# Kernel optimization log

Hardware: AMD Instinct MI355X
Metric: run time of the kernel (lower is better)

Reference implementation:

```python
import jax, jax.numpy as jnp
import numpy as np
from jax import lax

N = 4096
E = 131072
C = 128
CH = [(128, 256), (256, 512), (512, 512), (512, 256), (256, 128)]


def setup_inputs() -> dict:
    key = jax.random.key(0)
    ks = jax.random.split(key, 16)
    inp = {}
    inp["x"] = jax.random.normal(ks[0], (N, C), jnp.float32)
    src = jax.random.randint(ks[1], (E,), 0, N)
    dst = jax.random.randint(ks[2], (E,), 0, N)
    inp["edge_index"] = jnp.stack([src, dst]).astype(jnp.int32)
    for i, (ci, co) in enumerate(CH):
        inp[f"theta{i}"] = jax.random.normal(ks[3 + i], (ci, co), jnp.float32) / np.float32(np.sqrt(ci))
        inp[f"b{i}"] = jax.random.normal(ks[8 + i], (co,), jnp.float32) * 0.02
    inp["p1"] = jax.random.normal(ks[13], (256,), jnp.float32)
    inp["p2"] = jax.random.normal(ks[14], (512,), jnp.float32)
    return inp


def gcn(x, W, theta, b):
    """GCNConv with edge weights, dense-adjacency form.
    A_hat = W + I (self loops, weight 1); deg = row-sum of A_hat;
    out[i] = sum_{(r->i)} d^-1/2[r] * w * d^-1/2[i] * (x@theta)[r] + b."""
    n = W.shape[0]
    A = W + jnp.eye(n, dtype=W.dtype)
    deg = A.sum(axis=1)
    dinv = jnp.where(deg > 0, lax.rsqrt(deg), 0.0)
    An = dinv[:, None] * A * dinv[None, :]
    return An.T @ (x @ theta) + b


def augment_adj(W):
    """add_self_loops -> spspmm(A, A) -> remove_self_loops, dense form."""
    n = W.shape[0]
    A = W + jnp.eye(n, dtype=W.dtype)
    A2 = A @ A
    return A2 * (1.0 - jnp.eye(n, dtype=W.dtype))


def topk_pool(x, W, p, k):
    """TopKPooling (ratio fixed via static k, single graph)."""
    score = jnp.tanh((x @ p) / jnp.linalg.norm(p))
    vals, perm = lax.top_k(score, k)
    xp = x[perm] * vals[:, None]
    Wp = W[perm][:, perm]  # filter_adj on surviving nodes
    return xp, Wp, perm


def reference(x, edge_index, theta0, theta1, theta2, theta3, theta4,
              b0, b1, b2, b3, b4, p1, p2):
    n = x.shape[0]
    # dense weighted adjacency from edge list (edge_weight = ones, duplicates sum)
    W = jnp.zeros((n, n), x.dtype).at[edge_index[0], edge_index[1]].add(1.0)

    # down block 0
    x0 = jax.nn.relu(gcn(x, W, theta0, b0))                 # [N, 256]
    x1, W1, perm1 = topk_pool(x0, augment_adj(W), p1, n // 2)
    # down block 1
    x1b = jax.nn.relu(gcn(x1, W1, theta1, b1))              # [N/2, 512]
    x2, W2, perm2 = topk_pool(x1b, augment_adj(W1), p2, n // 4)
    # bottleneck block
    xb = jax.nn.relu(gcn(x2, W2, theta2, b2))               # [N/4, 512]
    summary = xb.mean(axis=0, keepdims=True)                # global_mean_pool, 1 graph
    # up block (i=3): edges[1]=W1, res=x1b, perm2
    up1 = jnp.zeros_like(x1b).at[perm2].set(xb)
    xu = jax.nn.relu(gcn(x1b + up1, W1, theta3, b3))        # [N/2, 256]
    # up block (i=4): edges[0]=W, res=x0, perm1
    up0 = jnp.zeros_like(x0).at[perm1].set(xu)
    xout = jax.nn.relu(gcn(x0 + up0, W, theta4, b4))        # [N, 128]
    return xout, summary
```

## Files before the change

kernel.cpp:

```cpp
#include <hip/hip_runtime.h>

#define N0 4096
#define P1K 2048
#define P2K 1024
#define SPLITS 4

typedef short bf16x8 __attribute__((ext_vector_type(8)));
typedef float f32x4 __attribute__((ext_vector_type(4)));

__device__ __forceinline__ unsigned short f2bf(float f) {
  unsigned int u = __float_as_uint(f);
  unsigned int r = (u + 0x7fff + ((u >> 16) & 1)) >> 16;
  return (unsigned short)r;
}
__device__ __forceinline__ float bf2f(unsigned short h) {
  unsigned int u = ((unsigned int)h) << 16;
  return __uint_as_float(u);
}

__device__ __forceinline__ float blockReduceSum256(float v) {
  __shared__ float sh[16];
  int lane = threadIdx.x & 63;
  int w = threadIdx.x >> 6;
#pragma unroll
  for (int o = 32; o > 0; o >>= 1) v += __shfl_down(v, o, 64);
  __syncthreads();
  if (lane == 0) sh[w] = v;
  __syncthreads();
  float r = 0.f;
  if (threadIdx.x == 0) {
    int nw = (blockDim.x + 63) >> 6;
    for (int i = 0; i < nw; ++i) r += sh[i];
  }
  return r;
}

__device__ __forceinline__ int blockScanExclusive(int v, volatile int* wsums) {
  int lane = threadIdx.x & 63, w = threadIdx.x >> 6;
  int x = v;
#pragma unroll
  for (int o = 1; o < 64; o <<= 1) {
    int y = __shfl_up(x, o, 64);
    if (lane >= o) x += y;
  }
  if (lane == 63) wsums[w] = x;
  __syncthreads();
  if (threadIdx.x < 64) {
    int nw = blockDim.x >> 6;
    int s = (threadIdx.x < nw) ? wsums[threadIdx.x] : 0;
#pragma unroll
    for (int o = 1; o < 16; o <<= 1) {
      int y = __shfl_up(s, o, 64);
      if (lane >= o) s += y;
    }
    if (threadIdx.x < nw) wsums[threadIdx.x] = s;
  }
  __syncthreads();
  int base = (w > 0) ? wsums[w - 1] : 0;
  __syncthreads();
  return base + x - v;
}

__global__ void count_edges(const int* __restrict__ src, const int* __restrict__ dst,
                            int* __restrict__ co, int* __restrict__ ci, int E) {
  int e = blockIdx.x * blockDim.x + threadIdx.x;
  if (e >= E) return;
  atomicAdd(&co[src[e]], 1);
  atomicAdd(&ci[dst[e]], 1);
}

__global__ __launch_bounds__(1024) void exscan_dual(const int* __restrict__ co,
                                                    const int* __restrict__ ci,
                                                    int* __restrict__ optr,
                                                    int* __restrict__ iptr,
                                                    float* __restrict__ dinv0) {
  __shared__ int ls[1024];
  const int* cnt = blockIdx.x ? ci : co;
  int* ptr = blockIdx.x ? iptr : optr;
  int t = threadIdx.x;
  int v0 = cnt[t * 4], v1 = cnt[t * 4 + 1], v2 = cnt[t * 4 + 2], v3 = cnt[t * 4 + 3];
  int s = v0 + v1 + v2 + v3;
  ls[t] = s;
  __syncthreads();
  for (int off = 1; off < 1024; off <<= 1) {
    int x = (t >= off) ? ls[t - off] : 0;
    __syncthreads();
    ls[t] += x;
    __syncthreads();
  }
  int ex = (t > 0) ? ls[t - 1] : 0;
  ptr[t * 4]     = ex;
  ptr[t * 4 + 1] = ex + v0;
  ptr[t * 4 + 2] = ex + v0 + v1;
  ptr[t * 4 + 3] = ex + v0 + v1 + v2;
  if (t == 1023) ptr[4096] = ex + s;
  if (blockIdx.x == 0) {
    dinv0[t * 4]     = rsqrtf((float)v0 + 1.f);
    dinv0[t * 4 + 1] = rsqrtf((float)v1 + 1.f);
    dinv0[t * 4 + 2] = rsqrtf((float)v2 + 1.f);
    dinv0[t * 4 + 3] = rsqrtf((float)v3 + 1.f);
  }
}

__global__ void fill_edges(const int* __restrict__ src, const int* __restrict__ dst,
                           const int* __restrict__ optr, const int* __restrict__ iptr,
                           int* __restrict__ fo, int* __restrict__ fi,
                           int* __restrict__ odst, int* __restrict__ isrc, int E) {
  int e = blockIdx.x * blockDim.x + threadIdx.x;
  if (e >= E) return;
  int s = src[e], d = dst[e];
  odst[optr[s] + atomicAdd(&fo[s], 1)] = d;
  isrc[iptr[d] + atomicAdd(&fi[d], 1)] = s;
}

__global__ void conv_T_all(const float* __restrict__ t0, const float* __restrict__ t1,
                           const float* __restrict__ t2, const float* __restrict__ t3,
                           const float* __restrict__ t4,
                           unsigned short* __restrict__ o0h, unsigned short* __restrict__ o0l,
                           unsigned short* __restrict__ o1h, unsigned short* __restrict__ o1l,
                           unsigned short* __restrict__ o2, unsigned short* __restrict__ o3,
                           unsigned short* __restrict__ o4) {
  int idx = blockIdx.x * 256 + threadIdx.x;
  if (idx < 32768) {
    int k = idx >> 8, n = idx & 255;
    float v = t0[idx];
    unsigned short h = f2bf(v);
    o0h[(size_t)n * 128 + k] = h;
    o0l[(size_t)n * 128 + k] = f2bf(v - bf2f(h));
  } else if (idx < 163840) {
    int i = idx - 32768;
    int k = i >> 9, n = i & 511;
    float v = t1[i];
    unsigned short h = f2bf(v);
    o1h[(size_t)n * 256 + k] = h;
    o1l[(size_t)n * 256 + k] = f2bf(v - bf2f(h));
  } else if (idx < 425984) {
    int i = idx - 163840;
    int k = i >> 9, n = i & 511;
    o2[(size_t)n * 512 + k] = f2bf(t2[i]);
  } else if (idx < 557056) {
    int i = idx - 425984;
    int k = i >> 8, n = i & 255;
    o3[(size_t)n * 512 + k] = f2bf(t3[i]);
  } else if (idx < 589824) {
    int i = idx - 557056;
    int k = i >> 7, n = i & 127;
    o4[(size_t)n * 256 + k] = f2bf(t4[i]);
  }
}

template <bool TOUT>
__global__ __launch_bounds__(256) void gemm3(const float* __restrict__ A,
                                             const unsigned short* __restrict__ BhT,
                                             const unsigned short* __restrict__ BlT,
                                             const int* __restrict__ permA,
                                             const float* __restrict__ valsA,
                                             const float* __restrict__ dinv,
                                             float* __restrict__ C,
                                             unsigned short* __restrict__ ChT,
                                             unsigned short* __restrict__ ClT,
                                             int M, int N, int K, int nbx) {
  __shared__ unsigned short U[16384];
  unsigned short* Ah = U;
  unsigned short* Al = U + 4096;
  unsigned short* Bh = U + 8192;
  unsigned short* Bl = U + 12288;
  int tid = threadIdx.x;
  int by = blockIdx.x / nbx, bx = blockIdx.x % nbx;
  int row0 = by << 6, col0 = bx << 6;
  int l = tid & 63, wv = tid >> 6;
  int wr = (wv >> 1) << 5, wc = (wv & 1) << 5;
  f32x4 acc[2][2] = {};
  for (int k0 = 0; k0 < K; k0 += 64) {
#pragma unroll
    for (int it = 0; it < 2; ++it) {
      int idx = (it << 8) + tid;
      int r = idx >> 3, c8 = idx & 7;
      int sw = c8 ^ (r & 7);
      int row = row0 + r;
      int srow = permA ? permA[row] : row;
      float vs = valsA ? valsA[row] : 1.f;
      const float* Af = A + (size_t)srow * K + k0 + (c8 << 3);
      float4 f0 = *(const float4*)Af;
      float4 f1 = *(const float4*)(Af + 4);
      float vv[8] = {f0.x * vs, f0.y * vs, f0.z * vs, f0.w * vs,
                     f1.x * vs, f1.y * vs, f1.z * vs, f1.w * vs};
      uint4 uh, ul;
      unsigned short hh[8], ll[8];
#pragma unroll
      for (int q = 0; q < 8; ++q) {
        hh[q] = f2bf(vv[q]);
        ll[q] = f2bf(vv[q] - bf2f(hh[q]));
      }
      uh.x = (unsigned)hh[0] | ((unsigned)hh[1] << 16);
      uh.y = (unsigned)hh[2] | ((unsigned)hh[3] << 16);
      uh.z = (unsigned)hh[4] | ((unsigned)hh[5] << 16);
      uh.w = (unsigned)hh[6] | ((unsigned)hh[7] << 16);
      ul.x = (unsigned)ll[0] | ((unsigned)ll[1] << 16);
      ul.y = (unsigned)ll[2] | ((unsigned)ll[3] << 16);
      ul.z = (unsigned)ll[4] | ((unsigned)ll[5] << 16);
      ul.w = (unsigned)ll[6] | ((unsigned)ll[7] << 16);
      ((uint4*)Ah)[(r << 3) + sw] = uh;
      ((uint4*)Al)[(r << 3) + sw] = ul;
      ((uint4*)Bh)[(r << 3) + sw] =
          *(const uint4*)(BhT + (size_t)(col0 + r) * K + k0 + (c8 << 3));
      ((uint4*)Bl)[(r << 3) + sw] =
          *(const uint4*)(BlT + (size_t)(col0 + r) * K + k0 + (c8 << 3));
    }
    __syncthreads();
#pragma unroll
    for (int kk2 = 0; kk2 < 2; ++kk2) {
      int ch = (kk2 << 2) + (l >> 4);
      int ra = wr + (l & 15), rb = ra + 16;
      int ca = wc + (l & 15), cb = ca + 16;
      int oa0 = (ra << 6) + ((ch ^ (ra & 7)) << 3);
      int oa1 = (rb << 6) + ((ch ^ (rb & 7)) << 3);
      int ob0 = (ca << 6) + ((ch ^ (ca & 7)) << 3);
      int ob1 = (cb << 6) + ((ch ^ (cb & 7)) << 3);
      bf16x8 ah0 = *(const bf16x8*)&Ah[oa0], ah1 = *(const bf16x8*)&Ah[oa1];
      bf16x8 al0 = *(const bf16x8*)&Al[oa0], al1 = *(const bf16x8*)&Al[oa1];
      bf16x8 bh0 = *(const bf16x8*)&Bh[ob0], bh1 = *(const bf16x8*)&Bh[ob1];
      bf16x8 bl0 = *(const bf16x8*)&Bl[ob0], bl1 = *(const bf16x8*)&Bl[ob1];
      acc[0][0] = __builtin_amdgcn_mfma_f32_16x16x32_bf16(ah0, bh0, acc[0][0], 0, 0, 0);
      acc[0][1] = __builtin_amdgcn_mfma_f32_16x16x32_bf16(ah0, bh1, acc[0][1], 0, 0, 0);
      acc[1][0] = __builtin_amdgcn_mfma_f32_16x16x32_bf16(ah1, bh0, acc[1][0], 0, 0, 0);
      acc[1][1] = __builtin_amdgcn_mfma_f32_16x16x32_bf16(ah1, bh1, acc[1][1], 0, 0, 0);
      acc[0][0] = __builtin_amdgcn_mfma_f32_16x16x32_bf16(ah0, bl0, acc[0][0], 0, 0, 0);
      acc[0][1] = __builtin_amdgcn_mfma_f32_16x16x32_bf16(ah0, bl1, acc[0][1], 0, 0, 0);
      acc[1][0] = __builtin_amdgcn_mfma_f32_16x16x32_bf16(ah1, bl0, acc[1][0], 0, 0, 0);
      acc[1][1] = __builtin_amdgcn_mfma_f32_16x16x32_bf16(ah1, bl1, acc[1][1], 0, 0, 0);
      acc[0][0] = __builtin_amdgcn_mfma_f32_16x16x32_bf16(al0, bh0, acc[0][0], 0, 0, 0);
      acc[0][1] = __builtin_amdgcn_mfma_f32_16x16x32_bf16(al0, bh1, acc[0][1], 0, 0, 0);
      acc[1][0] = __builtin_amdgcn_mfma_f32_16x16x32_bf16(al1, bh0, acc[1][0], 0, 0, 0);
      acc[1][1] = __builtin_amdgcn_mfma_f32_16x16x32_bf16(al1, bh1, acc[1][1], 0, 0, 0);
    }
    __syncthreads();
  }
  int lrow = (l >> 4) << 2, lcol = l & 15;
  float* tf = (float*)U;
#pragma unroll
  for (int i = 0; i < 2; ++i)
#pragma unroll
    for (int j = 0; j < 2; ++j) {
      int lc = wc + (j << 4) + lcol;
      int lr0 = wr + (i << 4) + lrow;
      int c = col0 + lc;
#pragma unroll
      for (int rg = 0; rg < 4; ++rg) {
        int lr = lr0 + rg;
        int r = row0 + lr;
        float dv = dinv ? dinv[r] : 1.f;
        float v = acc[i][j][rg] * dv;
        C[(size_t)r * N + c] = v;
        if (TOUT) tf[lr * 65 + lc] = v;
      }
    }
  if (TOUT) {
    __syncthreads();
    for (int it = 0; it < 16; ++it) {
      int idx = (it << 8) + tid;
      int rr = idx >> 6, cc = idx & 63;
      float v = tf[cc * 65 + rr];
      unsigned short h = f2bf(v);
      size_t o = (size_t)(col0 + rr) * M + row0 + cc;
      ChT[o] = h;
      ClT[o] = f2bf(v - bf2f(h));
    }
  }
}

template <bool ABF16>
__global__ __launch_bounds__(256) void gemm_sk(const void* __restrict__ Av,
                                               const unsigned short* __restrict__ BT,
                                               const int* __restrict__ permA,
                                               const float* __restrict__ valsA,
                                               float* __restrict__ Pf,
                                               int M, int N, int K, int nbx, int nb2d) {
  __shared__ unsigned short As[64 * 64];
  __shared__ unsigned short Bs[64 * 64];
  int tid = threadIdx.x;
  int s = blockIdx.x / nb2d;
  int r2 = blockIdx.x % nb2d;
  int by = r2 / nbx, bx = r2 % nbx;
  int row0 = by << 6, col0 = bx << 6;
  int kc = K / SPLITS;
  int ks = s * kc, ke = ks + kc;
  int l = tid & 63, wv = tid >> 6;
  int wr = (wv >> 1) << 5, wc = (wv & 1) << 5;
  f32x4 acc[2][2] = {};
  for (int k0 = ks; k0 < ke; k0 += 64) {
#pragma unroll
    for (int it = 0; it < 2; ++it) {
      int idx = (it << 8) + tid;
      int r = idx >> 3, c8 = idx & 7;
      int sw = c8 ^ (r & 7);
      if (ABF16) {
        ((uint4*)As)[(r << 3) + sw] =
            *(const uint4*)((const unsigned short*)Av + (size_t)(row0 + r) * K + k0 + (c8 << 3));
      } else {
        int row = row0 + r;
        int srow = permA ? permA[row] : row;
        float vs = valsA ? valsA[row] : 1.f;
        const float* Af = (const float*)Av + (size_t)srow * K + k0 + (c8 << 3);
        float4 f0 = *(const float4*)Af;
        float4 f1 = *(const float4*)(Af + 4);
        uint4 u;
        u.x = (unsigned)f2bf(f0.x * vs) | ((unsigned)f2bf(f0.y * vs) << 16);
        u.y = (unsigned)f2bf(f0.z * vs) | ((unsigned)f2bf(f0.w * vs) << 16);
        u.z = (unsigned)f2bf(f1.x * vs) | ((unsigned)f2bf(f1.y * vs) << 16);
        u.w = (unsigned)f2bf(f1.z * vs) | ((unsigned)f2bf(f1.w * vs) << 16);
        ((uint4*)As)[(r << 3) + sw] = u;
      }
      ((uint4*)Bs)[(r << 3) + sw] =
          *(const uint4*)(BT + (size_t)(col0 + r) * K + k0 + (c8 << 3));
    }
    __syncthreads();
#pragma unroll
    for (int kk2 = 0; kk2 < 2; ++kk2) {
      int ch = (kk2 << 2) + (l >> 4);
      int ra = wr + (l & 15), rb = ra + 16;
      int ca = wc + (l & 15), cb = ca + 16;
      bf16x8 a0 = *(const bf16x8*)&As[(ra << 6) + ((ch ^ (ra & 7)) << 3)];
      bf16x8 a1 = *(const bf16x8*)&As[(rb << 6) + ((ch ^ (rb & 7)) << 3)];
      bf16x8 b0 = *(const bf16x8*)&Bs[(ca << 6) + ((ch ^ (ca & 7)) << 3)];
      bf16x8 b1 = *(const bf16x8*)&Bs[(cb << 6) + ((ch ^ (cb & 7)) << 3)];
      acc[0][0] = __builtin_amdgcn_mfma_f32_16x16x32_bf16(a0, b0, acc[0][0], 0, 0, 0);
      acc[0][1] = __builtin_amdgcn_mfma_f32_16x16x32_bf16(a0, b1, acc[0][1], 0, 0, 0);
      acc[1][0] = __builtin_amdgcn_mfma_f32_16x16x32_bf16(a1, b0, acc[1][0], 0, 0, 0);
      acc[1][1] = __builtin_amdgcn_mfma_f32_16x16x32_bf16(a1, b1, acc[1][1], 0, 0, 0);
    }
    __syncthreads();
  }
  int lrow = (l >> 4) << 2, lcol = l & 15;
  float* P = Pf + (size_t)s * M * N;
#pragma unroll
  for (int i = 0; i < 2; ++i)
#pragma unroll
    for (int j = 0; j < 2; ++j) {
      int c = col0 + wc + (j << 4) + lcol;
      int r0 = row0 + wr + (i << 4) + lrow;
#pragma unroll
      for (int rg = 0; rg < 4; ++rg)
        P[(size_t)(r0 + rg) * N + c] = acc[i][j][rg];
    }
}

__global__ __launch_bounds__(256) void gemm_skd(const unsigned short* __restrict__ A,
                                                const unsigned short* __restrict__ BhT,
                                                const unsigned short* __restrict__ BlT,
                                                float* __restrict__ Pf,
                                                int M, int N, int K, int nbx, int nb2d) {
  __shared__ unsigned short As[4096], Bh[4096], Bl[4096];
  int tid = threadIdx.x;
  int s = blockIdx.x / nb2d;
  int r2 = blockIdx.x % nb2d;
  int by = r2 / nbx, bx = r2 % nbx;
  int row0 = by << 6, col0 = bx << 6;
  int kc = K / SPLITS;
  int ks = s * kc, ke = ks + kc;
  int l = tid & 63, wv = tid >> 6;
  int wr = (wv >> 1) << 5, wc = (wv & 1) << 5;
  f32x4 acc[2][2] = {};
  for (int k0 = ks; k0 < ke; k0 += 64) {
#pragma unroll
    for (int it = 0; it < 2; ++it) {
      int idx = (it << 8) + tid;
      int r = idx >> 3, c8 = idx & 7;
      int sw = c8 ^ (r & 7);
      ((uint4*)As)[(r << 3) + sw] =
          *(const uint4*)(A + (size_t)(row0 + r) * K + k0 + (c8 << 3));
      ((uint4*)Bh)[(r << 3) + sw] =
          *(const uint4*)(BhT + (size_t)(col0 + r) * K + k0 + (c8 << 3));
      ((uint4*)Bl)[(r << 3) + sw] =
          *(const uint4*)(BlT + (size_t)(col0 + r) * K + k0 + (c8 << 3));
    }
    __syncthreads();
#pragma unroll
    for (int kk2 = 0; kk2 < 2; ++kk2) {
      int ch = (kk2 << 2) + (l >> 4);
      int ra = wr + (l & 15), rb = ra + 16;
      int ca = wc + (l & 15), cb = ca + 16;
      bf16x8 a0 = *(const bf16x8*)&As[(ra << 6) + ((ch ^ (ra & 7)) << 3)];
      bf16x8 a1 = *(const bf16x8*)&As[(rb << 6) + ((ch ^ (rb & 7)) << 3)];
      bf16x8 bh0 = *(const bf16x8*)&Bh[(ca << 6) + ((ch ^ (ca & 7)) << 3)];
      bf16x8 bh1 = *(const bf16x8*)&Bh[(cb << 6) + ((ch ^ (cb & 7)) << 3)];
      bf16x8 bl0 = *(const bf16x8*)&Bl[(ca << 6) + ((ch ^ (ca & 7)) << 3)];
      bf16x8 bl1 = *(const bf16x8*)&Bl[(cb << 6) + ((ch ^ (cb & 7)) << 3)];
      acc[0][0] = __builtin_amdgcn_mfma_f32_16x16x32_bf16(a0, bh0, acc[0][0], 0, 0, 0);
      acc[0][1] = __builtin_amdgcn_mfma_f32_16x16x32_bf16(a0, bh1, acc[0][1], 0, 0, 0);
      acc[1][0] = __builtin_amdgcn_mfma_f32_16x16x32_bf16(a1, bh0, acc[1][0], 0, 0, 0);
      acc[1][1] = __builtin_amdgcn_mfma_f32_16x16x32_bf16(a1, bh1, acc[1][1], 0, 0, 0);
      acc[0][0] = __builtin_amdgcn_mfma_f32_16x16x32_bf16(a0, bl0, acc[0][0], 0, 0, 0);
      acc[0][1] = __builtin_amdgcn_mfma_f32_16x16x32_bf16(a0, bl1, acc[0][1], 0, 0, 0);
      acc[1][0] = __builtin_amdgcn_mfma_f32_16x16x32_bf16(a1, bl0, acc[1][0], 0, 0, 0);
      acc[1][1] = __builtin_amdgcn_mfma_f32_16x16x32_bf16(a1, bl1, acc[1][1], 0, 0, 0);
    }
    __syncthreads();
  }
  int lrow = (l >> 4) << 2, lcol = l & 15;
  float* P = Pf + (size_t)s * M * N;
#pragma unroll
  for (int i = 0; i < 2; ++i)
#pragma unroll
    for (int j = 0; j < 2; ++j) {
      int c = col0 + wc + (j << 4) + lcol;
      int r0 = row0 + wr + (i << 4) + lrow;
#pragma unroll
      for (int rg = 0; rg < 4; ++rg)
        P[(size_t)(r0 + rg) * N + c] = acc[i][j][rg];
    }
}

__global__ __launch_bounds__(256) void epi_red0_t(const float* __restrict__ Pf,
                                                  const float* __restrict__ dinv,
                                                  float* __restrict__ Cf,
                                                  unsigned short* __restrict__ CbT,
                                                  int M, int N, int dm) {
  __shared__ float t[64][65];
  int nbx = N >> 6;
  int by = blockIdx.x / nbx, bx = blockIdx.x % nbx;
  int r0 = by << 6, c0 = bx << 6;
  size_t MN = (size_t)M * N;
  for (int it = 0; it < 16; ++it) {
    int idx = (it << 8) + threadIdx.x;
    int r = idx >> 6, c = idx & 63;
    size_t o = (size_t)(r0 + r) * N + c0 + c;
    float v = 0.f;
#pragma unroll
    for (int s = 0; s < SPLITS; ++s) v += Pf[s * MN + o];
    float dv = 1.f;
    if (dm == 1) dv = dinv[r0 + r];
    else if (dm == 2) dv = rsqrtf(dinv[r0 + r] + 1.f);
    v *= dv;
    Cf[o] = v;
    t[r][c] = v;
  }
  __syncthreads();
  if (CbT) {
    for (int it = 0; it < 16; ++it) {
      int idx = (it << 8) + threadIdx.x;
      int rr = idx >> 6, cc = idx & 63;
      CbT[(size_t)(c0 + rr) * M + r0 + cc] = f2bf(t[cc][rr]);
    }
  }
}

__global__ __launch_bounds__(256) void epi_red1(const float* __restrict__ Pf,
                                                const float* __restrict__ Zadd,
                                                const float* __restrict__ dinv,
                                                const float* __restrict__ bias,
                                                const int* __restrict__ permS,
                                                float* __restrict__ scatterDst,
                                                float* __restrict__ outp, int M, int N,
                                                int dm) {
  int g = blockIdx.x * 256 + threadIdx.x;
  size_t base = (size_t)g * 4;
  size_t MN = (size_t)M * N;
  if (base >= MN) return;
  int r = (int)(base / N), c = (int)(base % N);
  float4 a = *(const float4*)&Pf[base];
#pragma unroll
  for (int s = 1; s < SPLITS; ++s) {
    float4 p = *(const float4*)&Pf[s * MN + base];
    a.x += p.x; a.y += p.y; a.z += p.z; a.w += p.w;
  }
  float4 z = *(const float4*)&Zadd[base];
  float dv = (dm == 2) ? rsqrtf(dinv[r] + 1.f) : dinv[r];
  float4 bb = *(const float4*)&bias[c];
  float4 o;
  o.x = fmaxf(dv * (a.x + z.x) + bb.x, 0.f);
  o.y = fmaxf(dv * (a.y + z.y) + bb.y, 0.f);
  o.z = fmaxf(dv * (a.z + z.z) + bb.z, 0.f);
  o.w = fmaxf(dv * (a.w + z.w) + bb.w, 0.f);
  if (outp) *(float4*)&outp[base] = o;
  if (permS) {
    float4* d = (float4*)&scatterDst[(size_t)permS[r] * N + c];
    float4 cur = *d;
    cur.x += o.x; cur.y += o.y; cur.z += o.z; cur.w += o.w;
    *d = cur;
  }
}

__global__ __launch_bounds__(256) void epi_red1s(const float* __restrict__ Pf,
                                                 const float* __restrict__ Zadd,
                                                 const float* __restrict__ dinv,
                                                 const float* __restrict__ bias,
                                                 const float* __restrict__ pvec,
                                                 float* __restrict__ sc,
                                                 float* __restrict__ outp) {
  __shared__ float shs[2][2][2];
  int li = threadIdx.x & 127;
  int lr = threadIdx.x >> 7;
  int r = blockIdx.x * 2 + lr;
  size_t base = (size_t)r * 512 + li * 4;
  const size_t MN = (size_t)2048 * 512;
  float4 a = *(const float4*)&Pf[base];
#pragma unroll
  for (int s = 1; s < SPLITS; ++s) {
    float4 p = *(const float4*)&Pf[s * MN + base];
    a.x += p.x; a.y += p.y; a.z += p.z; a.w += p.w;
  }
  float4 z = *(const float4*)&Zadd[base];
  float dv = dinv[r];
  float4 bb = *(const float4*)&bias[li * 4];
  float4 o;
  o.x = fmaxf(dv * (a.x + z.x) + bb.x, 0.f);
  o.y = fmaxf(dv * (a.y + z.y) + bb.y, 0.f);
  o.z = fmaxf(dv * (a.z + z.z) + bb.z, 0.f);
  o.w = fmaxf(dv * (a.w + z.w) + bb.w, 0.f);
  *(float4*)&outp[base] = o;
  float4 pv = *(const float4*)&pvec[li * 4];
  float s1 = pv.x * pv.x + pv.y * pv.y + pv.z * pv.z + pv.w * pv.w;
  float s2 = o.x * pv.x + o.y * pv.y + o.z * pv.z + o.w * pv.w;
#pragma unroll
  for (int t = 32; t > 0; t >>= 1) {
    s1 += __shfl_down(s1, t, 64);
    s2 += __shfl_down(s2, t, 64);
  }
  int wir = (threadIdx.x >> 6) & 1;
  if ((threadIdx.x & 63) == 0) { shs[lr][wir][0] = s1; shs[lr][wir][1] = s2; }
  __syncthreads();
  if ((threadIdx.x & 127) == 0) {
    float S1 = shs[lr][0][0] + shs[lr][1][0];
    float S2 = shs[lr][0][1] + shs[lr][1][1];
    sc[r] = tanhf(S2 / sqrtf(S1));
  }
}

__global__ __launch_bounds__(256) void mm_w2_mfma(const unsigned short* __restrict__ Wb,
                                                  const unsigned short* __restrict__ WbT,
                                                  const int* __restrict__ perm2,
                                                  float* __restrict__ W2f) {
  __shared__ unsigned short As[64 * 64];
  __shared__ unsigned short Bs[64 * 64];
  __shared__ int pr[64], pc[64];
  int tid = threadIdx.x;
  int s = blockIdx.x >> 8;
  int t2d = blockIdx.x & 255;
  int bx = t2d & 15, by = t2d >> 4;
  int row0 = by << 6, col0 = bx << 6;
  int ks = s * 512, ke = ks + 512;
  if (tid < 64) pr[tid] = perm2[row0 + tid];
  else if (tid < 128) pc[tid - 64] = perm2[col0 + tid - 128 + 64];
  __syncthreads();
  int l = tid & 63, wv = tid >> 6;
  int wr = (wv >> 1) << 5, wc = (wv & 1) << 5;
  f32x4 acc[2][2] = {};
  for (int k0 = ks; k0 < ke; k0 += 64) {
#pragma unroll
    for (int it = 0; it < 2; ++it) {
      int idx = (it << 8) + tid;
      int r = idx >> 3, c8 = idx & 7;
      int sw = c8 ^ (r & 7);
      ((uint4*)As)[(r << 3) + sw] =
          *(const uint4*)(Wb + (size_t)pr[r] * 2048 + k0 + (c8 << 3));
      ((uint4*)Bs)[(r << 3) + sw] =
          *(const uint4*)(WbT + (size_t)pc[r] * 2048 + k0 + (c8 << 3));
    }
    __syncthreads();
    if (tid < 64) {
      int r = tid, d = pr[r] - k0;
      if (d >= 0 && d < 64) {
        int ui = (r << 6) + (((d >> 3) ^ (r & 7)) << 3) + (d & 7);
        As[ui] = f2bf(bf2f(As[ui]) + 1.f);
      }
    } else if (tid < 128) {
      int c = tid - 64, d = pc[c] - k0;
      if (d >= 0 && d < 64) {
        int ui = (c << 6) + (((d >> 3) ^ (c & 7)) << 3) + (d & 7);
        Bs[ui] = f2bf(bf2f(Bs[ui]) + 1.f);
      }
    }
    __syncthreads();
#pragma unroll
    for (int kk2 = 0; kk2 < 2; ++kk2) {
      int ch = (kk2 << 2) + (l >> 4);
      int ra = wr + (l & 15), rb = ra + 16;
      int ca = wc + (l & 15), cb = ca + 16;
      bf16x8 a0 = *(const bf16x8*)&As[(ra << 6) + ((ch ^ (ra & 7)) << 3)];
      bf16x8 a1 = *(const bf16x8*)&As[(rb << 6) + ((ch ^ (rb & 7)) << 3)];
      bf16x8 b0 = *(const bf16x8*)&Bs[(ca << 6) + ((ch ^ (ca & 7)) << 3)];
      bf16x8 b1 = *(const bf16x8*)&Bs[(cb << 6) + ((ch ^ (cb & 7)) << 3)];
      acc[0][0] = __builtin_amdgcn_mfma_f32_16x16x32_bf16(a0, b0, acc[0][0], 0, 0, 0);
      acc[0][1] = __builtin_amdgcn_mfma_f32_16x16x32_bf16(a0, b1, acc[0][1], 0, 0, 0);
      acc[1][0] = __builtin_amdgcn_mfma_f32_16x16x32_bf16(a1, b0, acc[1][0], 0, 0, 0);
      acc[1][1] = __builtin_amdgcn_mfma_f32_16x16x32_bf16(a1, b1, acc[1][1], 0, 0, 0);
    }
    __syncthreads();
  }
  int lrow = (l >> 4) << 2, lcol = l & 15;
#pragma unroll
  for (int i = 0; i < 2; ++i)
#pragma unroll
    for (int j = 0; j < 2; ++j) {
      int c = col0 + wc + (j << 4) + lcol;
      int r0 = row0 + wr + (i << 4) + lrow;
#pragma unroll
      for (int rg = 0; rg < 4; ++rg)
        atomicAdd(&W2f[(size_t)(r0 + rg) * 1024 + c], acc[i][j][rg]);
    }
}

__global__ __launch_bounds__(256) void w2_post(const float* __restrict__ W2f,
                                               unsigned short* __restrict__ W2Tb,
                                               float* __restrict__ degsum2) {
  __shared__ float t[64][65];
  int bx = blockIdx.x & 15, by = blockIdx.x >> 4;
  int r0 = by << 6, c0 = bx << 6;
  for (int it = 0; it < 16; ++it) {
    int idx = (it << 8) + threadIdx.x;
    int r = idx >> 6, c = idx & 63;
    float v = W2f[(size_t)(r0 + r) * 1024 + c0 + c];
    if (r0 + r == c0 + c) v = 0.f;
    t[r][c] = v;
  }
  __syncthreads();
  if (threadIdx.x < 64) {
    float s = 0.f;
    for (int c = 0; c < 64; ++c) s += t[threadIdx.x][c];
    atomicAdd(&degsum2[r0 + threadIdx.x], s);
  }
  for (int it = 0; it < 16; ++it) {
    int idx = (it << 8) + threadIdx.x;
    int rr = idx >> 6, cc = idx & 63;
    W2Tb[(size_t)(c0 + rr) * 1024 + r0 + cc] = f2bf(t[cc][rr]);
  }
}

__global__ __launch_bounds__(256) void transpose_bf16(const unsigned short* __restrict__ in,
                                                      unsigned short* __restrict__ out,
                                                      int n) {
  __shared__ unsigned short t[64][65];
  int nb = n >> 6;
  int bx = blockIdx.x % nb, by = blockIdx.x / nb;
  int r0 = by << 6, c0 = bx << 6;
  for (int it = 0; it < 16; ++it) {
    int idx = (it << 8) + threadIdx.x;
    int r = idx >> 6, c = idx & 63;
    t[r][c] = in[(size_t)(r0 + r) * n + c0 + c];
  }
  __syncthreads();
  for (int it = 0; it < 16; ++it) {
    int idx = (it << 8) + threadIdx.x;
    int r = idx >> 6, c = idx & 63;
    out[(size_t)(c0 + r) * n + r0 + c] = t[c][r];
  }
}

template <int C, bool SCORE>
__global__ __launch_bounds__(256) void gcn_spmm4(const int* __restrict__ iptr,
                                                 const int* __restrict__ isrc,
                                                 const float* __restrict__ Z,
                                                 const float* __restrict__ dinv,
                                                 const float* __restrict__ bias,
                                                 const float* __restrict__ pvec,
                                                 float* __restrict__ sc,
                                                 float* __restrict__ outp) {
  constexpr int L = C / 4;
  int li = threadIdx.x % L;
  int i = blockIdx.x * (256 / L) + threadIdx.x / L;
  float4 acc = *(const float4*)(Z + (size_t)i * C + li * 4);
  int beg = iptr[i], end = iptr[i + 1];
  for (int e = beg; e < end; ++e) {
    float4 z = *(const float4*)(Z + (size_t)isrc[e] * C + li * 4);
    acc.x += z.x; acc.y += z.y; acc.z += z.z; acc.w += z.w;
  }
  float d = dinv[i];
  float4 bb = *(const float4*)(bias + li * 4);
  float4 o;
  o.x = fmaxf(d * acc.x + bb.x, 0.f);
  o.y = fmaxf(d * acc.y + bb.y, 0.f);
  o.z = fmaxf(d * acc.z + bb.z, 0.f);
  o.w = fmaxf(d * acc.w + bb.w, 0.f);
  *(float4*)(outp + (size_t)i * C + li * 4) = o;
  if (SCORE) {
    float4 pv = *(const float4*)(pvec + li * 4);
    float s1 = pv.x * pv.x + pv.y * pv.y + pv.z * pv.z + pv.w * pv.w;
    float s2 = o.x * pv.x + o.y * pv.y + o.z * pv.z + o.w * pv.w;
#pragma unroll
    for (int t = 32; t > 0; t >>= 1) {
      s1 += __shfl_down(s1, t, 64);
      s2 += __shfl_down(s2, t, 64);
    }
    if ((threadIdx.x & 63) == 0) sc[i] = tanhf(s2 / sqrtf(s1));
  }
}

__global__ __launch_bounds__(1024) void topk_select(const float* __restrict__ score,
                                                    int n, int k, int* __restrict__ perm,
                                                    float* __restrict__ vals,
                                                    int* __restrict__ rank) {
  __shared__ unsigned int keys[4096];
  __shared__ int hist[256];
  __shared__ int wsums[16];
  __shared__ unsigned int sh_prefix;
  __shared__ int sh_rem;
  int t = threadIdx.x;
  int m = n >> 10;
  for (int i = t; i < n; i += 1024) {
    unsigned int u = __float_as_uint(score[i]);
    keys[i] = u ^ ((unsigned int)((int)u >> 31) | 0x80000000u);
  }
  if (t == 0) { sh_prefix = 0u; sh_rem = k; }
  __syncthreads();
  for (int round = 0; round < 4; ++round) {
    int shift = 24 - (round << 3);
    if (t < 256) hist[t] = 0;
    __syncthreads();
    unsigned int prefix = sh_prefix;
    unsigned int maskhi = (round == 0) ? 0u : (0xFFFFFFFFu << (shift + 8));
    for (int i = t; i < n; i += 1024) {
      unsigned int kk = keys[i];
      if ((kk & maskhi) == prefix) atomicAdd(&hist[(kk >> shift) & 255], 1);
    }
    __syncthreads();
    if (t == 0) {
      int rem = sh_rem, acc = 0, b = 255;
      for (; b > 0; --b) {
        if (acc + hist[b] >= rem) break;
        acc += hist[b];
      }
      sh_rem = rem - acc;
      sh_prefix = prefix | ((unsigned int)b << shift);
    }
    __syncthreads();
  }
  unsigned int thr = sh_prefix;
  int need = sh_rem;
  int base = t * m;
  int f[4];
  int cnt = 0;
#pragma unroll
  for (int j = 0; j < 4; ++j) {
    f[j] = 0;
    if (j < m) { f[j] = (keys[base + j] == thr) ? 1 : 0; cnt += f[j]; }
  }
  int ex = blockScanExclusive(cnt, wsums);
  int sel[4];
  int scnt = 0;
#pragma unroll
  for (int j = 0; j < 4; ++j) {
    sel[j] = 0;
    if (j < m) {
      unsigned int kk = keys[base + j];
      sel[j] = (kk > thr) || (kk == thr && ex < need);
      ex += f[j];
      scnt += sel[j];
    }
  }
  int pos = blockScanExclusive(scnt, wsums);
#pragma unroll
  for (int j = 0; j < 4; ++j) {
    if (j < m) {
      int i = base + j;
      if (sel[j]) {
        unsigned int kk = keys[i];
        unsigned int u = (kk & 0x80000000u) ? (kk ^ 0x80000000u) : ~kk;
        perm[pos] = i;
        vals[pos] = __uint_as_float(u);
        rank[i] = pos;
        pos++;
      } else {
        rank[i] = -1;
      }
    }
  }
}

__global__ __launch_bounds__(256) void build_W1(const int* __restrict__ optr,
                                                const int* __restrict__ odst,
                                                const int* __restrict__ perm1,
                                                const int* __restrict__ rank1,
                                                unsigned short* __restrict__ W1b,
                                                float* __restrict__ dinv1) {
  __shared__ float row[2048];
  int a = blockIdx.x;
  int pa = perm1[a];
  for (int i = threadIdx.x; i < 2048; i += 256) row[i] = 0.f;
  __syncthreads();
  int kbeg = optr[pa], kend = optr[pa + 1];
  int nk = kend - kbeg + 1;
  int wv = threadIdx.x >> 6, lane = threadIdx.x & 63;
  for (int kidx = wv; kidx < nk; kidx += 4) {
    int k = (kidx == 0) ? pa : odst[kbeg + kidx - 1];
    int jbeg = optr[k], jend = optr[k + 1];
    for (int jj = jbeg - 1 + lane; jj < jend; jj += 64) {
      int j = (jj < jbeg) ? k : odst[jj];
      int rb = rank1[j];
      if (rb >= 0) atomicAdd(&row[rb], 1.0f);
    }
  }
  __syncthreads();
  float ssum = 0.f;
  for (int i = threadIdx.x; i < 2048; i += 256) {
    float v = (i == a) ? 0.f : row[i];
    W1b[(size_t)a * 2048 + i] = f2bf(v);
    ssum += v;
  }
  float t = blockReduceSum256(ssum);
  if (threadIdx.x == 0) dinv1[a] = rsqrtf(t + 1.0f);
}

__global__ void mean_cols(const float* __restrict__ X, int R, int C, float* __restrict__ outp) {
  int c = blockIdx.x;
  float s = 0.f;
  for (int r = threadIdx.x; r < R; r += blockDim.x) s += X[(size_t)r * C + c];
  float t = blockReduceSum256(s);
  if (threadIdx.x == 0) outp[c] = t / (float)R;
}

extern "C" void kernel_launch(void* const* d_in, const int* in_sizes, int n_in,
                              void* d_out, int out_size, void* d_ws, size_t ws_size,
                              hipStream_t stream) {
  const float* x      = (const float*)d_in[0];
  const int*   eidx   = (const int*)d_in[1];
  const float* theta0 = (const float*)d_in[2];
  const float* b0     = (const float*)d_in[3];
  const float* theta1 = (const float*)d_in[4];
  const float* b1     = (const float*)d_in[5];
  const float* theta2 = (const float*)d_in[6];
  const float* b2     = (const float*)d_in[7];
  const float* theta3 = (const float*)d_in[8];
  const float* b3     = (const float*)d_in[9];
  const float* theta4 = (const float*)d_in[10];
  const float* b4     = (const float*)d_in[11];
  const float* p1     = (const float*)d_in[12];
  const float* p2     = (const float*)d_in[13];
  const int E = in_sizes[1] / 2;
  const int* src = eidx;
  const int* dst = eidx + E;
  float* out = (float*)d_out;

  char* wsb = (char*)d_ws;
  size_t off = 0;
  auto alloc = [&](size_t bytes) -> void* {
    void* p = wsb + off;
    off = (off + bytes + 255) & ~(size_t)255;
    return p;
  };
  char* zblock = (char*)alloc((size_t)4 * N0 * 4 + P2K * 4 + (size_t)P2K * P2K * 4);
  int* cnt4 = (int*)zblock;
  float* degsum2 = (float*)(zblock + (size_t)4 * N0 * 4);
  float* W2f = (float*)(zblock + (size_t)4 * N0 * 4 + P2K * 4);
  size_t zbytes = (size_t)4 * N0 * 4 + P2K * 4 + (size_t)P2K * P2K * 4;

  int* optr  = (int*)alloc((N0 + 1) * 4);
  int* iptr  = (int*)alloc((N0 + 1) * 4);
  int* odst  = (int*)alloc((size_t)E * 4);
  int* isrc  = (int*)alloc((size_t)E * 4);
  int* perm1 = (int*)alloc(P1K * 4);
  int* rank1 = (int*)alloc(N0 * 4);
  int* perm2 = (int*)alloc(P2K * 4);
  int* rank2 = (int*)alloc(P1K * 4);
  float* dinv0 = (float*)alloc(N0 * 4);
  float* dinv1 = (float*)alloc(P1K * 4);
  float* vals1 = (float*)alloc(P1K * 4);
  float* vals2 = (float*)alloc(P2K * 4);
  float* score = (float*)alloc(N0 * 4);
  float* x0  = (float*)alloc((size_t)N0 * 256 * 4);
  float* x1b = (float*)alloc((size_t)P1K * 512 * 4);
  float* xb  = (float*)alloc((size_t)P2K * 512 * 4);
  float* SA  = (float*)alloc((size_t)P1K * 512 * 4);
  float* Pf  = (float*)alloc((size_t)SPLITS * 1048576 * 4);
  unsigned short* W1b  = (unsigned short*)alloc((size_t)P1K * P1K * 2);
  unsigned short* W1bT = (unsigned short*)alloc((size_t)P1K * P1K * 2);
  unsigned short* W2Tb = (unsigned short*)alloc((size_t)P2K * P2K * 2);
  unsigned short* SAbT = (unsigned short*)alloc((size_t)524288 * 2);
  unsigned short* ZhT  = (unsigned short*)alloc((size_t)512 * 2048 * 2);
  unsigned short* ZlT  = (unsigned short*)alloc((size_t)512 * 2048 * 2);
  unsigned short* t0hT = (unsigned short*)alloc((size_t)256 * 128 * 2);
  unsigned short* t0lT = (unsigned short*)alloc((size_t)256 * 128 * 2);
  unsigned short* t1hT = (unsigned short*)alloc((size_t)512 * 256 * 2);
  unsigned short* t1lT = (unsigned short*)alloc((size_t)512 * 256 * 2);
  unsigned short* t2T  = (unsigned short*)alloc((size_t)512 * 512 * 2);
  unsigned short* t3T  = (unsigned short*)alloc((size_t)256 * 512 * 2);
  unsigned short* t4T  = (unsigned short*)alloc((size_t)128 * 256 * 2);
  (void)ws_size; (void)n_in; (void)out_size;

  int* co = cnt4;
  int* ci = cnt4 + N0;
  int* fo = cnt4 + 2 * N0;
  int* fi = cnt4 + 3 * N0;

  hipMemsetAsync(zblock, 0, zbytes, stream);
  count_edges<<<E / 256, 256, 0, stream>>>(src, dst, co, ci, E);
  exscan_dual<<<2, 1024, 0, stream>>>(co, ci, optr, iptr, dinv0);
  fill_edges<<<E / 256, 256, 0, stream>>>(src, dst, optr, iptr, fo, fi, odst, isrc, E);
  conv_T_all<<<2304, 256, 0, stream>>>(theta0, theta1, theta2, theta3, theta4,
                                       t0hT, t0lT, t1hT, t1lT, t2T, t3T, t4T);

  gemm3<false><<<64 * 4, 256, 0, stream>>>(x, t0hT, t0lT, nullptr, nullptr, dinv0, SA,
                                           nullptr, nullptr, 4096, 256, 128, 4);
  gcn_spmm4<256, true><<<1024, 256, 0, stream>>>(iptr, isrc, SA, dinv0, b0, p1, score, x0);

  topk_select<<<1, 1024, 0, stream>>>(score, 4096, 2048, perm1, vals1, rank1);
  build_W1<<<2048, 256, 0, stream>>>(optr, odst, perm1, rank1, W1b, dinv1);
  transpose_bf16<<<(2048 / 64) * (2048 / 64), 256, 0, stream>>>(W1b, W1bT, 2048);

  gemm3<true><<<32 * 8, 256, 0, stream>>>(x0, t1hT, t1lT, perm1, vals1, dinv1, SA,
                                          ZhT, ZlT, 2048, 512, 256, 8);
  gemm_skd<<<256 * SPLITS, 256, 0, stream>>>(W1bT, ZhT, ZlT, Pf, 2048, 512, 2048, 8, 256);
  epi_red1s<<<1024, 256, 0, stream>>>(Pf, SA, dinv1, b1, p2, score, x1b);

  topk_select<<<1, 1024, 0, stream>>>(score, 2048, 1024, perm2, vals2, rank2);
  mm_w2_mfma<<<256 * SPLITS, 256, 0, stream>>>(W1b, W1bT, perm2, W2f);
  w2_post<<<256, 256, 0, stream>>>(W2f, W2Tb, degsum2);

  gemm_sk<false><<<128 * SPLITS, 256, 0, stream>>>(x1b, t2T, perm2, vals2, Pf,
                                                   1024, 512, 512, 8, 128);
  epi_red0_t<<<128, 256, 0, stream>>>(Pf, degsum2, SA, SAbT, 1024, 512, 2);
  gemm_sk<true><<<128 * SPLITS, 256, 0, stream>>>(W2Tb, SAbT, nullptr, nullptr, Pf,
                                                  1024, 512, 1024, 8, 128);
  epi_red1<<<1024 * 512 / 1024, 256, 0, stream>>>(Pf, SA, degsum2, b2, perm2, x1b, xb,
                                                  1024, 512, 2);
  mean_cols<<<512, 256, 0, stream>>>(xb, 1024, 512, out + 524288);

  gemm_sk<false><<<128 * SPLITS, 256, 0, stream>>>(x1b, t3T, nullptr, nullptr, Pf,
                                                   2048, 256, 512, 4, 128);
  epi_red0_t<<<128, 256, 0, stream>>>(Pf, dinv1, SA, SAbT, 2048, 256, 1);
  gemm_sk<true><<<128 * SPLITS, 256, 0, stream>>>(W1bT, SAbT, nullptr, nullptr, Pf,
                                                  2048, 256, 2048, 4, 128);
  epi_red1<<<2048 * 256 / 1024, 256, 0, stream>>>(Pf, SA, dinv1, b3, perm1, x0, nullptr,
                                                  2048, 256, 1);

  gemm_sk<false><<<128 * SPLITS, 256, 0, stream>>>(x0, t4T, nullptr, nullptr, Pf,
                                                   4096, 128, 256, 2, 128);
  epi_red0_t<<<128, 256, 0, stream>>>(Pf, dinv0, SA, nullptr, 4096, 128, 1);
  gcn_spmm4<128, false><<<512, 256, 0, stream>>>(iptr, isrc, SA, dinv0, b4, nullptr, nullptr,
                                                 out);
}
```

Before: 331.3 us.

## Fuse independent kernels via block-index dispatch and drop split-K for small GEMMs

Independent stages are merged into single launches that pick their work by block index: edge counting with the theta conversion, edge fill with the first GEMM, the transpose with the second GEMM, the W2 product with the bottleneck feature GEMM, and the column mean with the up-block feature GEMM. The small feature GEMMs that used split-K plus a separate reduction/epilogue kernel now use a non-split GEMM with the dinv scaling and transposed bf16 output fused into the epilogue, and a new w2T kernel produces dinv2 directly. This removes many launches and partial-sum round trips through memory. In exchange, mixed-role kernels carry the larger shared-memory and register footprint of their heaviest body, which can lower occupancy, and the non-split GEMMs launch fewer blocks.

```diff
diff --git a/kernel.cpp b/kernel.cpp
--- a/kernel.cpp
+++ b/kernel.cpp
@@ -61,66 +61,30 @@
   return base + x - v;
 }
 
-__global__ void count_edges(const int* __restrict__ src, const int* __restrict__ dst,
-                            int* __restrict__ co, int* __restrict__ ci, int E) {
-  int e = blockIdx.x * blockDim.x + threadIdx.x;
-  if (e >= E) return;
-  atomicAdd(&co[src[e]], 1);
-  atomicAdd(&ci[dst[e]], 1);
-}
-
-__global__ __launch_bounds__(1024) void exscan_dual(const int* __restrict__ co,
-                                                    const int* __restrict__ ci,
-                                                    int* __restrict__ optr,
-                                                    int* __restrict__ iptr,
-                                                    float* __restrict__ dinv0) {
-  __shared__ int ls[1024];
-  const int* cnt = blockIdx.x ? ci : co;
-  int* ptr = blockIdx.x ? iptr : optr;
-  int t = threadIdx.x;
-  int v0 = cnt[t * 4], v1 = cnt[t * 4 + 1], v2 = cnt[t * 4 + 2], v3 = cnt[t * 4 + 3];
-  int s = v0 + v1 + v2 + v3;
-  ls[t] = s;
-  __syncthreads();
-  for (int off = 1; off < 1024; off <<= 1) {
-    int x = (t >= off) ? ls[t - off] : 0;
-    __syncthreads();
-    ls[t] += x;
-    __syncthreads();
-  }
-  int ex = (t > 0) ? ls[t - 1] : 0;
-  ptr[t * 4]     = ex;
-  ptr[t * 4 + 1] = ex + v0;
-  ptr[t * 4 + 2] = ex + v0 + v1;
-  ptr[t * 4 + 3] = ex + v0 + v1 + v2;
-  if (t == 1023) ptr[4096] = ex + s;
-  if (blockIdx.x == 0) {
-    dinv0[t * 4]     = rsqrtf((float)v0 + 1.f);
-    dinv0[t * 4 + 1] = rsqrtf((float)v1 + 1.f);
-    dinv0[t * 4 + 2] = rsqrtf((float)v2 + 1.f);
-    dinv0[t * 4 + 3] = rsqrtf((float)v3 + 1.f);
-  }
-}
-
-__global__ void fill_edges(const int* __restrict__ src, const int* __restrict__ dst,
-                           const int* __restrict__ optr, const int* __restrict__ iptr,
-                           int* __restrict__ fo, int* __restrict__ fi,
-                           int* __restrict__ odst, int* __restrict__ isrc, int E) {
-  int e = blockIdx.x * blockDim.x + threadIdx.x;
-  if (e >= E) return;
-  int s = src[e], d = dst[e];
-  odst[optr[s] + atomicAdd(&fo[s], 1)] = d;
-  isrc[iptr[d] + atomicAdd(&fi[d], 1)] = s;
-}
-
-__global__ void conv_T_all(const float* __restrict__ t0, const float* __restrict__ t1,
-                           const float* __restrict__ t2, const float* __restrict__ t3,
-                           const float* __restrict__ t4,
-                           unsigned short* __restrict__ o0h, unsigned short* __restrict__ o0l,
-                           unsigned short* __restrict__ o1h, unsigned short* __restrict__ o1l,
-                           unsigned short* __restrict__ o2, unsigned short* __restrict__ o3,
-                           unsigned short* __restrict__ o4) {
-  int idx = blockIdx.x * 256 + threadIdx.x;
+__device__ __forceinline__ void count_edges_body(int b, const int* __restrict__ src,
+                                                 const int* __restrict__ dst,
+                                                 int* __restrict__ co, int* __restrict__ ci,
+                                                 int E) {
+  int e = b * 256 + threadIdx.x;
+  if (e < E) {
+    atomicAdd(&co[src[e]], 1);
+    atomicAdd(&ci[dst[e]], 1);
+  }
+}
+
+__device__ __forceinline__ void conv_body(int b, const float* __restrict__ t0,
+                                          const float* __restrict__ t1,
+                                          const float* __restrict__ t2,
+                                          const float* __restrict__ t3,
+                                          const float* __restrict__ t4,
+                                          unsigned short* __restrict__ o0h,
+                                          unsigned short* __restrict__ o0l,
+                                          unsigned short* __restrict__ o1h,
+                                          unsigned short* __restrict__ o1l,
+                                          unsigned short* __restrict__ o2,
+                                          unsigned short* __restrict__ o3,
+                                          unsigned short* __restrict__ o4) {
+  int idx = b * 256 + threadIdx.x;
   if (idx < 32768) {
     int k = idx >> 8, n = idx & 255;
     float v = t0[idx];
@@ -149,24 +113,79 @@
   }
 }
 
+__global__ __launch_bounds__(256) void fused_ce_conv(
+    const int* __restrict__ src, const int* __restrict__ dst, int* __restrict__ co,
+    int* __restrict__ ci, int E, const float* t0, const float* t1, const float* t2,
+    const float* t3, const float* t4, unsigned short* o0h, unsigned short* o0l,
+    unsigned short* o1h, unsigned short* o1l, unsigned short* o2, unsigned short* o3,
+    unsigned short* o4) {
+  if (blockIdx.x < 512) count_edges_body(blockIdx.x, src, dst, co, ci, E);
+  else conv_body(blockIdx.x - 512, t0, t1, t2, t3, t4, o0h, o0l, o1h, o1l, o2, o3, o4);
+}
+
+__global__ __launch_bounds__(1024) void exscan_dual(const int* __restrict__ co,
+                                                    const int* __restrict__ ci,
+                                                    int* __restrict__ optr,
+                                                    int* __restrict__ iptr,
+                                                    float* __restrict__ dinv0) {
+  __shared__ int ls[1024];
+  const int* cnt = blockIdx.x ? ci : co;
+  int* ptr = blockIdx.x ? iptr : optr;
+  int t = threadIdx.x;
+  int v0 = cnt[t * 4], v1 = cnt[t * 4 + 1], v2 = cnt[t * 4 + 2], v3 = cnt[t * 4 + 3];
+  int s = v0 + v1 + v2 + v3;
+  ls[t] = s;
+  __syncthreads();
+  for (int off = 1; off < 1024; off <<= 1) {
+    int x = (t >= off) ? ls[t - off] : 0;
+    __syncthreads();
+    ls[t] += x;
+    __syncthreads();
+  }
+  int ex = (t > 0) ? ls[t - 1] : 0;
+  ptr[t * 4]     = ex;
+  ptr[t * 4 + 1] = ex + v0;
+  ptr[t * 4 + 2] = ex + v0 + v1;
+  ptr[t * 4 + 3] = ex + v0 + v1 + v2;
+  if (t == 1023) ptr[4096] = ex + s;
+  if (blockIdx.x == 0) {
+    dinv0[t * 4]     = rsqrtf((float)v0 + 1.f);
+    dinv0[t * 4 + 1] = rsqrtf((float)v1 + 1.f);
+    dinv0[t * 4 + 2] = rsqrtf((float)v2 + 1.f);
+    dinv0[t * 4 + 3] = rsqrtf((float)v3 + 1.f);
+  }
+}
+
+__device__ __forceinline__ void fill_body(int b, const int* __restrict__ src,
+                                          const int* __restrict__ dst,
+                                          const int* __restrict__ optr,
+                                          const int* __restrict__ iptr,
+                                          int* __restrict__ fo, int* __restrict__ fi,
+                                          int* __restrict__ odst, int* __restrict__ isrc,
+                                          int E) {
+  int e = b * 256 + threadIdx.x;
+  if (e < E) {
+    int s = src[e], d = dst[e];
+    odst[optr[s] + atomicAdd(&fo[s], 1)] = d;
+    isrc[iptr[d] + atomicAdd(&fi[d], 1)] = s;
+  }
+}
+
 template <bool TOUT>
-__global__ __launch_bounds__(256) void gemm3(const float* __restrict__ A,
-                                             const unsigned short* __restrict__ BhT,
-                                             const unsigned short* __restrict__ BlT,
-                                             const int* __restrict__ permA,
-                                             const float* __restrict__ valsA,
-                                             const float* __restrict__ dinv,
-                                             float* __restrict__ C,
-                                             unsigned short* __restrict__ ChT,
-                                             unsigned short* __restrict__ ClT,
-                                             int M, int N, int K, int nbx) {
+__device__ void gemm3_body(int bid, const float* __restrict__ A,
+                           const unsigned short* __restrict__ BhT,
+                           const unsigned short* __restrict__ BlT,
+                           const int* __restrict__ permA, const float* __restrict__ valsA,
+                           const float* __restrict__ dinv, float* __restrict__ C,
+                           unsigned short* __restrict__ ChT, unsigned short* __restrict__ ClT,
+                           int M, int N, int K, int nbx) {
   __shared__ unsigned short U[16384];
   unsigned short* Ah = U;
   unsigned short* Al = U + 4096;
   unsigned short* Bh = U + 8192;
   unsigned short* Bl = U + 12288;
   int tid = threadIdx.x;
-  int by = blockIdx.x / nbx, bx = blockIdx.x % nbx;
+  int by = bid / nbx, bx = bid % nbx;
   int row0 = by << 6, col0 = bx << 6;
   int l = tid & 63, wv = tid >> 6;
   int wr = (wv >> 1) << 5, wc = (wv & 1) << 5;
@@ -269,80 +288,42 @@
   }
 }
 
-template <bool ABF16>
-__global__ __launch_bounds__(256) void gemm_sk(const void* __restrict__ Av,
-                                               const unsigned short* __restrict__ BT,
-                                               const int* __restrict__ permA,
-                                               const float* __restrict__ valsA,
-                                               float* __restrict__ Pf,
-                                               int M, int N, int K, int nbx, int nb2d) {
-  __shared__ unsigned short As[64 * 64];
-  __shared__ unsigned short Bs[64 * 64];
-  int tid = threadIdx.x;
-  int s = blockIdx.x / nb2d;
-  int r2 = blockIdx.x % nb2d;
-  int by = r2 / nbx, bx = r2 % nbx;
-  int row0 = by << 6, col0 = bx << 6;
-  int kc = K / SPLITS;
-  int ks = s * kc, ke = ks + kc;
-  int l = tid & 63, wv = tid >> 6;
-  int wr = (wv >> 1) << 5, wc = (wv & 1) << 5;
-  f32x4 acc[2][2] = {};
-  for (int k0 = ks; k0 < ke; k0 += 64) {
-#pragma unroll
-    for (int it = 0; it < 2; ++it) {
-      int idx = (it << 8) + tid;
-      int r = idx >> 3, c8 = idx & 7;
-      int sw = c8 ^ (r & 7);
-      if (ABF16) {
-        ((uint4*)As)[(r << 3) + sw] =
-            *(const uint4*)((const unsigned short*)Av + (size_t)(row0 + r) * K + k0 + (c8 << 3));
-      } else {
-        int row = row0 + r;
-        int srow = permA ? permA[row] : row;
-        float vs = valsA ? valsA[row] : 1.f;
-        const float* Af = (const float*)Av + (size_t)srow * K + k0 + (c8 << 3);
-        float4 f0 = *(const float4*)Af;
-        float4 f1 = *(const float4*)(Af + 4);
-        uint4 u;
-        u.x = (unsigned)f2bf(f0.x * vs) | ((unsigned)f2bf(f0.y * vs) << 16);
-        u.y = (unsigned)f2bf(f0.z * vs) | ((unsigned)f2bf(f0.w * vs) << 16);
-        u.z = (unsigned)f2bf(f1.x * vs) | ((unsigned)f2bf(f1.y * vs) << 16);
-        u.w = (unsigned)f2bf(f1.z * vs) | ((unsigned)f2bf(f1.w * vs) << 16);
-        ((uint4*)As)[(r << 3) + sw] = u;
-      }
-      ((uint4*)Bs)[(r << 3) + sw] =
-          *(const uint4*)(BT + (size_t)(col0 + r) * K + k0 + (c8 << 3));
-    }
-    __syncthreads();
-#pragma unroll
-    for (int kk2 = 0; kk2 < 2; ++kk2) {
-      int ch = (kk2 << 2) + (l >> 4);
-      int ra = wr + (l & 15), rb = ra + 16;
-      int ca = wc + (l & 15), cb = ca + 16;
-      bf16x8 a0 = *(const bf16x8*)&As[(ra << 6) + ((ch ^ (ra & 7)) << 3)];
-      bf16x8 a1 = *(const bf16x8*)&As[(rb << 6) + ((ch ^ (rb & 7)) << 3)];
-      bf16x8 b0 = *(const bf16x8*)&Bs[(ca << 6) + ((ch ^ (ca & 7)) << 3)];
-      bf16x8 b1 = *(const bf16x8*)&Bs[(cb << 6) + ((ch ^ (cb & 7)) << 3)];
-      acc[0][0] = __builtin_amdgcn_mfma_f32_16x16x32_bf16(a0, b0, acc[0][0], 0, 0, 0);
-      acc[0][1] = __builtin_amdgcn_mfma_f32_16x16x32_bf16(a0, b1, acc[0][1], 0, 0, 0);
-      acc[1][0] = __builtin_amdgcn_mfma_f32_16x16x32_bf16(a1, b0, acc[1][0], 0, 0, 0);
-      acc[1][1] = __builtin_amdgcn_mfma_f32_16x16x32_bf16(a1, b1, acc[1][1], 0, 0, 0);
-    }
-    __syncthreads();
-  }
-  int lrow = (l >> 4) << 2, lcol = l & 15;
-  float* P = Pf + (size_t)s * M * N;
-#pragma unroll
-  for (int i = 0; i < 2; ++i)
-#pragma unroll
-    for (int j = 0; j < 2; ++j) {
-      int c = col0 + wc + (j << 4) + lcol;
-      int r0 = row0 + wr + (i << 4) + lrow;
-#pragma unroll
-      for (int rg = 0; rg < 4; ++rg)
-        P[(size_t)(r0 + rg) * N + c] = acc[i][j][rg];
-    }
+__global__ __launch_bounds__(256) void fused_fill_g3(
+    const int* src, const int* dst, const int* optr, const int* iptr, int* fo, int* fi,
+    int* odst, int* isrc, int E, const float* x, const unsigned short* t0hT,
+    const unsigned short* t0lT, const float* dinv0, float* SA) {
+  if (blockIdx.x < 512) fill_body(blockIdx.x, src, dst, optr, iptr, fo, fi, odst, isrc, E);
+  else gemm3_body<false>(blockIdx.x - 512, x, t0hT, t0lT, nullptr, nullptr, dinv0, SA,
+                         nullptr, nullptr, 4096, 256, 128, 4);
+}
+
+__device__ void transpose_body(int bid, const unsigned short* __restrict__ in,
+                               unsigned short* __restrict__ out, int n) {
+  __shared__ unsigned short t[64][65];
+  int nb = n >> 6;
+  int bx = bid % nb, by = bid / nb;
+  int r0 = by << 6, c0 = bx << 6;
+  for (int it = 0; it < 16; ++it) {
+    int idx = (it << 8) + threadIdx.x;
+    int r = idx >> 6, c = idx & 63;
+    t[r][c] = in[(size_t)(r0 + r) * n + c0 + c];
+  }
+  __syncthreads();
+  for (int it = 0; it < 16; ++it) {
+    int idx = (it << 8) + threadIdx.x;
+    int r = idx >> 6, c = idx & 63;
+    out[(size_t)(c0 + r) * n + r0 + c] = t[c][r];
+  }
+}
+
+__global__ __launch_bounds__(256) void fused_tr_g3(
+    const unsigned short* W1b, unsigned short* W1bT, const float* x0,
+    const unsigned short* t1hT, const unsigned short* t1lT, const int* perm1,
+    const float* vals1, const float* dinv1, float* SA, unsigned short* ZhT,
+    unsigned short* ZlT) {
+  if (blockIdx.x < 1024) transpose_body(blockIdx.x, W1b, W1bT, 2048);
+  else gemm3_body<true>(blockIdx.x - 1024, x0, t1hT, t1lT, perm1, vals1, dinv1, SA,
+                        ZhT, ZlT, 2048, 512, 256, 8);
 }
 
 __global__ __launch_bounds__(256) void gemm_skd(const unsigned short* __restrict__ A,
@@ -411,37 +392,276 @@
     }
 }
 
-__global__ __launch_bounds__(256) void epi_red0_t(const float* __restrict__ Pf,
-                                                  const float* __restrict__ dinv,
-                                                  float* __restrict__ Cf,
-                                                  unsigned short* __restrict__ CbT,
-                                                  int M, int N, int dm) {
+__global__ __launch_bounds__(256) void gemm_sk(const unsigned short* __restrict__ A,
+                                               const unsigned short* __restrict__ BT,
+                                               float* __restrict__ Pf,
+                                               int M, int N, int K, int nbx, int nb2d) {
+  __shared__ unsigned short As[4096];
+  __shared__ unsigned short Bs[4096];
+  int tid = threadIdx.x;
+  int s = blockIdx.x / nb2d;
+  int r2 = blockIdx.x % nb2d;
+  int by = r2 / nbx, bx = r2 % nbx;
+  int row0 = by << 6, col0 = bx << 6;
+  int kc = K / SPLITS;
+  int ks = s * kc, ke = ks + kc;
+  int l = tid & 63, wv = tid >> 6;
+  int wr = (wv >> 1) << 5, wc = (wv & 1) << 5;
+  f32x4 acc[2][2] = {};
+  for (int k0 = ks; k0 < ke; k0 += 64) {
+#pragma unroll
+    for (int it = 0; it < 2; ++it) {
+      int idx = (it << 8) + tid;
+      int r = idx >> 3, c8 = idx & 7;
+      int sw = c8 ^ (r & 7);
+      ((uint4*)As)[(r << 3) + sw] =
+          *(const uint4*)(A + (size_t)(row0 + r) * K + k0 + (c8 << 3));
+      ((uint4*)Bs)[(r << 3) + sw] =
+          *(const uint4*)(BT + (size_t)(col0 + r) * K + k0 + (c8 << 3));
+    }
+    __syncthreads();
+#pragma unroll
+    for (int kk2 = 0; kk2 < 2; ++kk2) {
+      int ch = (kk2 << 2) + (l >> 4);
+      int ra = wr + (l & 15), rb = ra + 16;
+      int ca = wc + (l & 15), cb = ca + 16;
+      bf16x8 a0 = *(const bf16x8*)&As[(ra << 6) + ((ch ^ (ra & 7)) << 3)];
+      bf16x8 a1 = *(const bf16x8*)&As[(rb << 6) + ((ch ^ (rb & 7)) << 3)];
+      bf16x8 b0 = *(const bf16x8*)&Bs[(ca << 6) + ((ch ^ (ca & 7)) << 3)];
+      bf16x8 b1 = *(const bf16x8*)&Bs[(cb << 6) + ((ch ^ (cb & 7)) << 3)];
+      acc[0][0] = __builtin_amdgcn_mfma_f32_16x16x32_bf16(a0, b0, acc[0][0], 0, 0, 0);
+      acc[0][1] = __builtin_amdgcn_mfma_f32_16x16x32_bf16(a0, b1, acc[0][1], 0, 0, 0);
+      acc[1][0] = __builtin_amdgcn_mfma_f32_16x16x32_bf16(a1, b0, acc[1][0], 0, 0, 0);
+      acc[1][1] = __builtin_amdgcn_mfma_f32_16x16x32_bf16(a1, b1, acc[1][1], 0, 0, 0);
+    }
+    __syncthreads();
+  }
+  int lrow = (l >> 4) << 2, lcol = l & 15;
+  float* P = Pf + (size_t)s * M * N;
+#pragma unroll
+  for (int i = 0; i < 2; ++i)
+#pragma unroll
+    for (int j = 0; j < 2; ++j) {
+      int c = col0 + wc + (j << 4) + lcol;
+      int r0 = row0 + wr + (i << 4) + lrow;
+#pragma unroll
+      for (int rg = 0; rg < 4; ++rg)
+        P[(size_t)(r0 + rg) * N + c] = acc[i][j][rg];
+    }
+}
+
+__device__ void gemm_e_body(int bid, const float* __restrict__ A,
+                            const unsigned short* __restrict__ BT,
+                            const int* __restrict__ permA, const float* __restrict__ valsA,
+                            const float* __restrict__ dinv, int dm,
+                            float* __restrict__ Cf, unsigned short* __restrict__ CbT,
+                            int M, int N, int K, int nbx) {
+  __shared__ char gsm[16640];
+  unsigned short* As = (unsigned short*)gsm;
+  unsigned short* Bs = (unsigned short*)(gsm + 8192);
+  int tid = threadIdx.x;
+  int by = bid / nbx, bx = bid % nbx;
+  int row0 = by << 6, col0 = bx << 6;
+  int l = tid & 63, wv = tid >> 6;
+  int wr = (wv >> 1) << 5, wc = (wv & 1) << 5;
+  f32x4 acc[2][2] = {};
+  for (int k0 = 0; k0 < K; k0 += 64) {
+#pragma unroll
+    for (int it = 0; it < 2; ++it) {
+      int idx = (it << 8) + tid;
+      int r = idx >> 3, c8 = idx & 7;
+      int sw = c8 ^ (r & 7);
+      int row = row0 + r;
+      int srow = permA ? permA[row] : row;
+      float vs = valsA ? valsA[row] : 1.f;
+      const float* Af = A + (size_t)srow * K + k0 + (c8 << 3);
+      float4 f0 = *(const float4*)Af;
+      float4 f1 = *(const float4*)(Af + 4);
+      uint4 u;
+      u.x = (unsigned)f2bf(f0.x * vs) | ((unsigned)f2bf(f0.y * vs) << 16);
+      u.y = (unsigned)f2bf(f0.z * vs) | ((unsigned)f2bf(f0.w * vs) << 16);
+      u.z = (unsigned)f2bf(f1.x * vs) | ((unsigned)f2bf(f1.y * vs) << 16);
+      u.w = (unsigned)f2bf(f1.z * vs) | ((unsigned)f2bf(f1.w * vs) << 16);
+      ((uint4*)As)[(r << 3) + sw] = u;
+      ((uint4*)Bs)[(r << 3) + sw] =
+          *(const uint4*)(BT + (size_t)(col0 + r) * K + k0 + (c8 << 3));
+    }
+    __syncthreads();
+#pragma unroll
+    for (int kk2 = 0; kk2 < 2; ++kk2) {
+      int ch = (kk2 << 2) + (l >> 4);
+      int ra = wr + (l & 15), rb = ra + 16;
+      int ca = wc + (l & 15), cb = ca + 16;
+      bf16x8 a0 = *(const bf16x8*)&As[(ra << 6) + ((ch ^ (ra & 7)) << 3)];
+      bf16x8 a1 = *(const bf16x8*)&As[(rb << 6) + ((ch ^ (rb & 7)) << 3)];
+      bf16x8 b0 = *(const bf16x8*)&Bs[(ca << 6) + ((ch ^ (ca & 7)) << 3)];
+      bf16x8 b1 = *(const bf16x8*)&Bs[(cb << 6) + ((ch ^ (cb & 7)) << 3)];
+      acc[0][0] = __builtin_amdgcn_mfma_f32_16x16x32_bf16(a0, b0, acc[0][0], 0, 0, 0);
+      acc[0][1] = __builtin_amdgcn_mfma_f32_16x16x32_bf16(a0, b1, acc[0][1], 0, 0, 0);
+      acc[1][0] = __builtin_amdgcn_mfma_f32_16x16x32_bf16(a1, b0, acc[1][0], 0, 0, 0);
+      acc[1][1] = __builtin_amdgcn_mfma_f32_16x16x32_bf16(a1, b1, acc[1][1], 0, 0, 0);
+    }
+    __syncthreads();
+  }
+  int lrow = (l >> 4) << 2, lcol = l & 15;
+  float* tf = (float*)gsm;
+#pragma unroll
+  for (int i = 0; i < 2; ++i)
+#pragma unroll
+    for (int j = 0; j < 2; ++j) {
+      int lc = wc + (j << 4) + lcol;
+      int lr0 = wr + (i << 4) + lrow;
+      int c = col0 + lc;
+#pragma unroll
+      for (int rg = 0; rg < 4; ++rg) {
+        int lr = lr0 + rg;
+        int r = row0 + lr;
+        float dv = (dm == 1) ? dinv[r] : 1.f;
+        float v = acc[i][j][rg] * dv;
+        Cf[(size_t)r * N + c] = v;
+        if (CbT) tf[lr * 65 + lc] = v;
+      }
+    }
+  if (CbT) {
+    __syncthreads();
+    for (int it = 0; it < 16; ++it) {
+      int idx = (it << 8) + tid;
+      int rr = idx >> 6, cc = idx & 63;
+      CbT[(size_t)(col0 + rr) * M + row0 + cc] = f2bf(tf[cc * 65 + rr]);
+    }
+  }
+}
+
+__global__ __launch_bounds__(256) void gemm_e_k(const float* A, const unsigned short* BT,
+                                                const int* permA, const float* valsA,
+                                                const float* dinv, int dm, float* Cf,
+                                                unsigned short* CbT, int M, int N, int K,
+                                                int nbx) {
+  gemm_e_body(blockIdx.x, A, BT, permA, valsA, dinv, dm, Cf, CbT, M, N, K, nbx);
+}
+
+__device__ void mm_w2_body(int bid, const unsigned short* __restrict__ Wb,
+                           const unsigned short* __restrict__ WbT,
+                           const int* __restrict__ perm2, float* __restrict__ W2f,
+                           float* __restrict__ degsum2) {
+  __shared__ unsigned short As[4096];
+  __shared__ unsigned short Bs[4096];
+  __shared__ int pr[64], pc[64];
+  int tid = threadIdx.x;
+  int s = bid >> 8;
+  int t2d = bid & 255;
+  int bx = t2d & 15, by = t2d >> 4;
+  int row0 = by << 6, col0 = bx << 6;
+  int ks = s * 512, ke = ks + 512;
+  if (tid < 64) pr[tid] = perm2[row0 + tid];
+  else if (tid < 128) pc[tid - 64] = perm2[col0 + tid - 128 + 64];
+  __syncthreads();
+  int l = tid & 63, wv = tid >> 6;
+  int wr = (wv >> 1) << 5, wc = (wv & 1) << 5;
+  f32x4 acc[2][2] = {};
+  for (int k0 = ks; k0 < ke; k0 += 64) {
+#pragma unroll
+    for (int it = 0; it < 2; ++it) {
+      int idx = (it << 8) + tid;
+      int r = idx >> 3, c8 = idx & 7;
+      int sw = c8 ^ (r & 7);
+      ((uint4*)As)[(r << 3) + sw] =
+          *(const uint4*)(Wb + (size_t)pr[r] * 2048 + k0 + (c8 << 3));
+      ((uint4*)Bs)[(r << 3) + sw] =
+          *(const uint4*)(WbT + (size_t)pc[r] * 2048 + k0 + (c8 << 3));
+    }
+    __syncthreads();
+    if (tid < 64) {
+      int r = tid, d = pr[r] - k0;
+      if (d >= 0 && d < 64) {
+        int ui = (r << 6) + (((d >> 3) ^ (r & 7)) << 3) + (d & 7);
+        As[ui] = f2bf(bf2f(As[ui]) + 1.f);
+      }
+    } else if (tid < 128) {
+      int c = tid - 64, d = pc[c] - k0;
+      if (d >= 0 && d < 64) {
+        int ui = (c << 6) + (((d >> 3) ^ (c & 7)) << 3) + (d & 7);
+        Bs[ui] = f2bf(bf2f(Bs[ui]) + 1.f);
+      }
+    }
+    __syncthreads();
+#pragma unroll
+    for (int kk2 = 0; kk2 < 2; ++kk2) {
+      int ch = (kk2 << 2) + (l >> 4);
+      int ra = wr + (l & 15), rb = ra + 16;
+      int ca = wc + (l & 15), cb = ca + 16;
+      bf16x8 a0 = *(const bf16x8*)&As[(ra << 6) + ((ch ^ (ra & 7)) << 3)];
+      bf16x8 a1 = *(const bf16x8*)&As[(rb << 6) + ((ch ^ (rb & 7)) << 3)];
+      bf16x8 b0 = *(const bf16x8*)&Bs[(ca << 6) + ((ch ^ (ca & 7)) << 3)];
+      bf16x8 b1 = *(const bf16x8*)&Bs[(cb << 6) + ((ch ^ (cb & 7)) << 3)];
+      acc[0][0] = __builtin_amdgcn_mfma_f32_16x16x32_bf16(a0, b0, acc[0][0], 0, 0, 0);
+      acc[0][1] = __builtin_amdgcn_mfma_f32_16x16x32_bf16(a0, b1, acc[0][1], 0, 0, 0);
+      acc[1][0] = __builtin_amdgcn_mfma_f32_16x16x32_bf16(a1, b0, acc[1][0], 0, 0, 0);
+      acc[1][1] = __builtin_amdgcn_mfma_f32_16x16x32_bf16(a1, b1, acc[1][1], 0, 0, 0);
+    }
+    __syncthreads();
+  }
+  int lrow = (l >> 4) << 2, lcol = l & 15;
+#pragma unroll
+  for (int i = 0; i < 2; ++i)
+#pragma unroll
+    for (int j = 0; j < 2; ++j) {
+      int c = col0 + wc + (j << 4) + lcol;
+      int r0 = row0 + wr + (i << 4) + lrow;
+#pragma unroll
+      for (int rg = 0; rg < 4; ++rg)
+        atomicAdd(&W2f[(size_t)(r0 + rg) * 1024 + c], acc[i][j][rg]);
+    }
+#pragma unroll
+  for (int i = 0; i < 2; ++i)
+#pragma unroll
+    for (int rg = 0; rg < 4; ++rg) {
+      float rs = acc[i][0][rg] + acc[i][1][rg];
+#pragma unroll
+      for (int o = 1; o < 16; o <<= 1) rs += __shfl_xor(rs, o, 64);
+      if ((l & 15) == 0) {
+        int r = row0 + wr + (i << 4) + lrow + rg;
+        atomicAdd(&degsum2[r], rs);
+      }
+    }
+}
+
+__global__ __launch_bounds__(256) void fused_w2_g2a(
+    const unsigned short* Wb, const unsigned short* WbT, const int* perm2, float* W2f,
+    float* degsum2, const float* x1b, const unsigned short* t2T, const float* vals2,
+    float* SA, unsigned short* SAbT) {
+  if (blockIdx.x < 1024) mm_w2_body(blockIdx.x, Wb, WbT, perm2, W2f, degsum2);
+  else gemm_e_body(blockIdx.x - 1024, x1b, t2T, perm2, vals2, nullptr, 0, SA, SAbT,
+                   1024, 512, 512, 8);
+}
+
+__global__ __launch_bounds__(256) void w2T(const float* __restrict__ W2f,
+                                           const float* __restrict__ degsum2,
+                                           unsigned short* __restrict__ W2Tb,
+                                           float* __restrict__ dinv2v) {
   __shared__ float t[64][65];
-  int nbx = N >> 6;
-  int by = blockIdx.x / nbx, bx = blockIdx.x % nbx;
+  __shared__ float ds[64];
+  int bx = blockIdx.x & 15, by = blockIdx.x >> 4;
   int r0 = by << 6, c0 = bx << 6;
-  size_t MN = (size_t)M * N;
+  if (threadIdx.x < 64) {
+    int r = r0 + threadIdx.x;
+    float dg = degsum2[r] - W2f[(size_t)r * 1024 + r];
+    float dv = rsqrtf(dg + 1.f);
+    ds[threadIdx.x] = dv;
+    if (bx == 0) dinv2v[r] = dv;
+  }
   for (int it = 0; it < 16; ++it) {
     int idx = (it << 8) + threadIdx.x;
     int r = idx >> 6, c = idx & 63;
-    size_t o = (size_t)(r0 + r) * N + c0 + c;
-    float v = 0.f;
-#pragma unroll
-    for (int s = 0; s < SPLITS; ++s) v += Pf[s * MN + o];
-    float dv = 1.f;
-    if (dm == 1) dv = dinv[r0 + r];
-    else if (dm == 2) dv = rsqrtf(dinv[r0 + r] + 1.f);
-    v *= dv;
-    Cf[o] = v;
+    float v = W2f[(size_t)(r0 + r) * 1024 + c0 + c];
+    if (r0 + r == c0 + c) v = 0.f;
     t[r][c] = v;
   }
   __syncthreads();
-  if (CbT) {
-    for (int it = 0; it < 16; ++it) {
-      int idx = (it << 8) + threadIdx.x;
-      int rr = idx >> 6, cc = idx & 63;
-      CbT[(size_t)(c0 + rr) * M + r0 + cc] = f2bf(t[cc][rr]);
-    }
+  for (int it = 0; it < 16; ++it) {
+    int idx = (it << 8) + threadIdx.x;
+    int rr = idx >> 6, cc = idx & 63;
+    W2Tb[(size_t)(c0 + rr) * 1024 + r0 + cc] = f2bf(t[cc][rr] * ds[cc]);
   }
 }
 
@@ -452,7 +672,7 @@
                                                 const int* __restrict__ permS,
                                                 float* __restrict__ scatterDst,
                                                 float* __restrict__ outp, int M, int N,
-                                                int dm) {
+                                                int zs) {
   int g = blockIdx.x * 256 + threadIdx.x;
   size_t base = (size_t)g * 4;
   size_t MN = (size_t)M * N;
@@ -465,13 +685,14 @@
     a.x += p.x; a.y += p.y; a.z += p.z; a.w += p.w;
   }
   float4 z = *(const float4*)&Zadd[base];
-  float dv = (dm == 2) ? rsqrtf(dinv[r] + 1.f) : dinv[r];
+  float dv = dinv[r];
+  float zf = zs ? dv : 1.f;
   float4 bb = *(const float4*)&bias[c];
   float4 o;
-  o.x = fmaxf(dv * (a.x + z.x) + bb.x, 0.f);
-  o.y = fmaxf(dv * (a.y + z.y) + bb.y, 0.f);
-  o.z = fmaxf(dv * (a.z + z.z) + bb.z, 0.f);
-  o.w = fmaxf(dv * (a.w + z.w) + bb.w, 0.f);
+  o.x = fmaxf(dv * (a.x + zf * z.x) + bb.x, 0.f);
+  o.y = fmaxf(dv * (a.y + zf * z.y) + bb.y, 0.f);
+  o.z = fmaxf(dv * (a.z + zf * z.z) + bb.z, 0.f);
+  o.w = fmaxf(dv * (a.w + zf * z.w) + bb.w, 0.f);
   if (outp) *(float4*)&outp[base] = o;
   if (permS) {
     float4* d = (float4*)&scatterDst[(size_t)permS[r] * N + c];
@@ -524,126 +745,6 @@
     float S1 = shs[lr][0][0] + shs[lr][1][0];
     float S2 = shs[lr][0][1] + shs[lr][1][1];
     sc[r] = tanhf(S2 / sqrtf(S1));
-  }
-}
-
-__global__ __launch_bounds__(256) void mm_w2_mfma(const unsigned short* __restrict__ Wb,
-                                                  const unsigned short* __restrict__ WbT,
-                                                  const int* __restrict__ perm2,
-                                                  float* __restrict__ W2f) {
-  __shared__ unsigned short As[64 * 64];
-  __shared__ unsigned short Bs[64 * 64];
-  __shared__ int pr[64], pc[64];
-  int tid = threadIdx.x;
-  int s = blockIdx.x >> 8;
-  int t2d = blockIdx.x & 255;
-  int bx = t2d & 15, by = t2d >> 4;
-  int row0 = by << 6, col0 = bx << 6;
-  int ks = s * 512, ke = ks + 512;
-  if (tid < 64) pr[tid] = perm2[row0 + tid];
-  else if (tid < 128) pc[tid - 64] = perm2[col0 + tid - 128 + 64];
-  __syncthreads();
-  int l = tid & 63, wv = tid >> 6;
-  int wr = (wv >> 1) << 5, wc = (wv & 1) << 5;
-  f32x4 acc[2][2] = {};
-  for (int k0 = ks; k0 < ke; k0 += 64) {
-#pragma unroll
-    for (int it = 0; it < 2; ++it) {
-      int idx = (it << 8) + tid;
-      int r = idx >> 3, c8 = idx & 7;
-      int sw = c8 ^ (r & 7);
-      ((uint4*)As)[(r << 3) + sw] =
-          *(const uint4*)(Wb + (size_t)pr[r] * 2048 + k0 + (c8 << 3));
-      ((uint4*)Bs)[(r << 3) + sw] =
-          *(const uint4*)(WbT + (size_t)pc[r] * 2048 + k0 + (c8 << 3));
-    }
-    __syncthreads();
-    if (tid < 64) {
-      int r = tid, d = pr[r] - k0;
-      if (d >= 0 && d < 64) {
-        int ui = (r << 6) + (((d >> 3) ^ (r & 7)) << 3) + (d & 7);
-        As[ui] = f2bf(bf2f(As[ui]) + 1.f);
-      }
-    } else if (tid < 128) {
-      int c = tid - 64, d = pc[c] - k0;
-      if (d >= 0 && d < 64) {
-        int ui = (c << 6) + (((d >> 3) ^ (c & 7)) << 3) + (d & 7);
-        Bs[ui] = f2bf(bf2f(Bs[ui]) + 1.f);
-      }
-    }
-    __syncthreads();
-#pragma unroll
-    for (int kk2 = 0; kk2 < 2; ++kk2) {
-      int ch = (kk2 << 2) + (l >> 4);
-      int ra = wr + (l & 15), rb = ra + 16;
-      int ca = wc + (l & 15), cb = ca + 16;
-      bf16x8 a0 = *(const bf16x8*)&As[(ra << 6) + ((ch ^ (ra & 7)) << 3)];
-      bf16x8 a1 = *(const bf16x8*)&As[(rb << 6) + ((ch ^ (rb & 7)) << 3)];
-      bf16x8 b0 = *(const bf16x8*)&Bs[(ca << 6) + ((ch ^ (ca & 7)) << 3)];
-      bf16x8 b1 = *(const bf16x8*)&Bs[(cb << 6) + ((ch ^ (cb & 7)) << 3)];
-      acc[0][0] = __builtin_amdgcn_mfma_f32_16x16x32_bf16(a0, b0, acc[0][0], 0, 0, 0);
-      acc[0][1] = __builtin_amdgcn_mfma_f32_16x16x32_bf16(a0, b1, acc[0][1], 0, 0, 0);
-      acc[1][0] = __builtin_amdgcn_mfma_f32_16x16x32_bf16(a1, b0, acc[1][0], 0, 0, 0);
-      acc[1][1] = __builtin_amdgcn_mfma_f32_16x16x32_bf16(a1, b1, acc[1][1], 0, 0, 0);
-    }
-    __syncthreads();
-  }
-  int lrow = (l >> 4) << 2, lcol = l & 15;
-#pragma unroll
-  for (int i = 0; i < 2; ++i)
-#pragma unroll
-    for (int j = 0; j < 2; ++j) {
-      int c = col0 + wc + (j << 4) + lcol;
-      int r0 = row0 + wr + (i << 4) + lrow;
-#pragma unroll
-      for (int rg = 0; rg < 4; ++rg)
-        atomicAdd(&W2f[(size_t)(r0 + rg) * 1024 + c], acc[i][j][rg]);
-    }
-}
-
-__global__ __launch_bounds__(256) void w2_post(const float* __restrict__ W2f,
-                                               unsigned short* __restrict__ W2Tb,
-                                               float* __restrict__ degsum2) {
-  __shared__ float t[64][65];
-  int bx = blockIdx.x & 15, by = blockIdx.x >> 4;
-  int r0 = by << 6, c0 = bx << 6;
-  for (int it = 0; it < 16; ++it) {
-    int idx = (it << 8) + threadIdx.x;
-    int r = idx >> 6, c = idx & 63;
-    float v = W2f[(size_t)(r0 + r) * 1024 + c0 + c];
-    if (r0 + r == c0 + c) v = 0.f;
-    t[r][c] = v;
-  }
-  __syncthreads();
-  if (threadIdx.x < 64) {
-    float s = 0.f;
-    for (int c = 0; c < 64; ++c) s += t[threadIdx.x][c];
-    atomicAdd(&degsum2[r0 + threadIdx.x], s);
-  }
-  for (int it = 0; it < 16; ++it) {
-    int idx = (it << 8) + threadIdx.x;
-    int rr = idx >> 6, cc = idx & 63;
-    W2Tb[(size_t)(c0 + rr) * 1024 + r0 + cc] = f2bf(t[cc][rr]);
-  }
-}
-
-__global__ __launch_bounds__(256) void transpose_bf16(const unsigned short* __restrict__ in,
-                                                      unsigned short* __restrict__ out,
-                                                      int n) {
-  __shared__ unsigned short t[64][65];
-  int nb = n >> 6;
-  int bx = blockIdx.x % nb, by = blockIdx.x / nb;
-  int r0 = by << 6, c0 = bx << 6;
-  for (int it = 0; it < 16; ++it) {
-    int idx = (it << 8) + threadIdx.x;
-    int r = idx >> 6, c = idx & 63;
-    t[r][c] = in[(size_t)(r0 + r) * n + c0 + c];
-  }
-  __syncthreads();
-  for (int it = 0; it < 16; ++it) {
-    int idx = (it << 8) + threadIdx.x;
-    int r = idx >> 6, c = idx & 63;
-    out[(size_t)(c0 + r) * n + r0 + c] = t[c][r];
   }
 }
 
@@ -801,12 +902,20 @@
   if (threadIdx.x == 0) dinv1[a] = rsqrtf(t + 1.0f);
 }
 
-__global__ void mean_cols(const float* __restrict__ X, int R, int C, float* __restrict__ outp) {
-  int c = blockIdx.x;
+__device__ void mean_cols_body(int c, const float* __restrict__ X, int R, int C,
+                               float* __restrict__ outp) {
   float s = 0.f;
-  for (int r = threadIdx.x; r < R; r += blockDim.x) s += X[(size_t)r * C + c];
+  for (int r = threadIdx.x; r < R; r += 256) s += X[(size_t)r * C + c];
   float t = blockReduceSum256(s);
   if (threadIdx.x == 0) outp[c] = t / (float)R;
+}
+
+__global__ __launch_bounds__(256) void fused_mean_up1a(
+    const float* xb, float* meanOut, const float* x1b, const unsigned short* t3T,
+    const float* dinv1, float* SA, unsigned short* SAbT) {
+  if (blockIdx.x < 512) mean_cols_body(blockIdx.x, xb, 1024, 512, meanOut);
+  else gemm_e_body(blockIdx.x - 512, x1b, t3T, nullptr, nullptr, dinv1, 1, SA, SAbT,
+                   2048, 256, 512, 4);
 }
 
 extern "C" void kernel_launch(void* const* d_in, const int* in_sizes, int n_in,
@@ -854,6 +963,7 @@
   int* rank2 = (int*)alloc(P1K * 4);
   float* dinv0 = (float*)alloc(N0 * 4);
   float* dinv1 = (float*)alloc(P1K * 4);
+  float* dinv2v = (float*)alloc(P2K * 4);
   float* vals1 = (float*)alloc(P1K * 4);
   float* vals2 = (float*)alloc(P2K * 4);
   float* score = (float*)alloc(N0 * 4);
@@ -883,49 +993,39 @@
   int* fi = cnt4 + 3 * N0;
 
   hipMemsetAsync(zblock, 0, zbytes, stream);
-  count_edges<<<E / 256, 256, 0, stream>>>(src, dst, co, ci, E);
+  fused_ce_conv<<<512 + 2304, 256, 0, stream>>>(src, dst, co, ci, E, theta0, theta1,
+                                                theta2, theta3, theta4, t0hT, t0lT,
+                                                t1hT, t1lT, t2T, t3T, t4T);
   exscan_dual<<<2, 1024, 0, stream>>>(co, ci, optr, iptr, dinv0);
-  fill_edges<<<E / 256, 256, 0, stream>>>(src, dst, optr, iptr, fo, fi, odst, isrc, E);
-  conv_T_all<<<2304, 256, 0, stream>>>(theta0, theta1, theta2, theta3, theta4,
-                                       t0hT, t0lT, t1hT, t1lT, t2T, t3T, t4T);
-
-  gemm3<false><<<64 * 4, 256, 0, stream>>>(x, t0hT, t0lT, nullptr, nullptr, dinv0, SA,
-                                           nullptr, nullptr, 4096, 256, 128, 4);
+  fused_fill_g3<<<512 + 256, 256, 0, stream>>>(src, dst, optr, iptr, fo, fi, odst, isrc,
+                                               E, x, t0hT, t0lT, dinv0, SA);
   gcn_spmm4<256, true><<<1024, 256, 0, stream>>>(iptr, isrc, SA, dinv0, b0, p1, score, x0);
 
   topk_select<<<1, 1024, 0, stream>>>(score, 4096, 2048, perm1, vals1, rank1);
   build_W1<<<2048, 256, 0, stream>>>(optr, odst, perm1, rank1, W1b, dinv1);
-  transpose_bf16<<<(2048 / 64) * (2048 / 64), 256, 0, stream>>>(W1b, W1bT, 2048);
-
-  gemm3<true><<<32 * 8, 256, 0, stream>>>(x0, t1hT, t1lT, perm1, vals1, dinv1, SA,
-                                          ZhT, ZlT, 2048, 512, 256, 8);
+  fused_tr_g3<<<1024 + 256, 256, 0, stream>>>(W1b, W1bT, x0, t1hT, t1lT, perm1, vals1,
+                                              dinv1, SA, ZhT, ZlT);
+
   gemm_skd<<<256 * SPLITS, 256, 0, stream>>>(W1bT, ZhT, ZlT, Pf, 2048, 512, 2048, 8, 256);
   epi_red1s<<<1024, 256, 0, stream>>>(Pf, SA, dinv1, b1, p2, score, x1b);
 
   topk_select<<<1, 1024, 0, stream>>>(score, 2048, 1024, perm2, vals2, rank2);
-  mm_w2_mfma<<<256 * SPLITS, 256, 0, stream>>>(W1b, W1bT, perm2, W2f);
-  w2_post<<<256, 256, 0, stream>>>(W2f, W2Tb, degsum2);
-
-  gemm_sk<false><<<128 * SPLITS, 256, 0, stream>>>(x1b, t2T, perm2, vals2, Pf,
-                                                   1024, 512, 512, 8, 128);
-  epi_red0_t<<<128, 256, 0, stream>>>(Pf, degsum2, SA, SAbT, 1024, 512, 2);
-  gemm_sk<true><<<128 * SPLITS, 256, 0, stream>>>(W2Tb, SAbT, nullptr, nullptr, Pf,
-                                                  1024, 512, 1024, 8, 128);
-  epi_red1<<<1024 * 512 / 1024, 256, 0, stream>>>(Pf, SA, degsum2, b2, perm2, x1b, xb,
-                                                  1024, 512, 2);
-  mean_cols<<<512, 256, 0, stream>>>(xb, 1024, 512, out + 524288);
-
-  gemm_sk<false><<<128 * SPLITS, 256, 0, stream>>>(x1b, t3T, nullptr, nullptr, Pf,
-                                                   2048, 256, 512, 4, 128);
-  epi_red0_t<<<128, 256, 0, stream>>>(Pf, dinv1, SA, SAbT, 2048, 256, 1);
-  gemm_sk<true><<<128 * SPLITS, 256, 0, stream>>>(W1bT, SAbT, nullptr, nullptr, Pf,
-                                                  2048, 256, 2048, 4, 128);
+  fused_w2_g2a<<<1024 + 128, 256, 0, stream>>>(W1b, W1bT, perm2, W2f, degsum2, x1b, t2T,
+                                               vals2, SA, SAbT);
+  w2T<<<256, 256, 0, stream>>>(W2f, degsum2, W2Tb, dinv2v);
+
+  gemm_sk<<<128 * SPLITS, 256, 0, stream>>>(W2Tb, SAbT, Pf, 1024, 512, 1024, 8, 128);
+  epi_red1<<<1024 * 512 / 1024, 256, 0, stream>>>(Pf, SA, dinv2v, b2, perm2, x1b, xb,
+                                                  1024, 512, 1);
+  fused_mean_up1a<<<512 + 128, 256, 0, stream>>>(xb, out + 524288, x1b, t3T, dinv1,
+                                                 SA, SAbT);
+
+  gemm_sk<<<128 * SPLITS, 256, 0, stream>>>(W1bT, SAbT, Pf, 2048, 256, 2048, 4, 128);
   epi_red1<<<2048 * 256 / 1024, 256, 0, stream>>>(Pf, SA, dinv1, b3, perm1, x0, nullptr,
-                                                  2048, 256, 1);
-
-  gemm_sk<false><<<128 * SPLITS, 256, 0, stream>>>(x0, t4T, nullptr, nullptr, Pf,
-                                                   4096, 128, 256, 2, 128);
-  epi_red0_t<<<128, 256, 0, stream>>>(Pf, dinv0, SA, nullptr, 4096, 128, 1);
-  gcn_spmm4<128, false><<<512, 256, 0, stream>>>(iptr, isrc, SA, dinv0, b4, nullptr, nullptr,
-                                                 out);
-}
+                                                  2048, 256, 0);
+
+  gemm_e_k<<<128, 256, 0, stream>>>(x0, t4T, nullptr, nullptr, dinv0, 1, SA, nullptr,
+                                    4096, 128, 256, 2);
+  gcn_spmm4<128, false><<<512, 256, 0, stream>>>(iptr, isrc, SA, dinv0, b4, nullptr,
+                                                 nullptr, out);
+}
```

After: 310.1 us. -6.4%, faster.
